# Optimization experiments

Measured on AMD Instinct MI355X. Metric: run time of the kernel, lower is better.

## Reference

```python
import jax, jax.numpy as jnp
import numpy as np
from jax import lax

B, S, D, H, L = 2, 2048, 512, 512, 2
M, NC, K, NH, WIN = 64, 16, 4, 8, 256
MAX_LR = 0.1


def setup_inputs() -> dict:
    key = jax.random.key(0)
    keys = iter(jax.random.split(key, 40))
    def nrm(shape, scale=0.02):
        return jax.random.normal(next(keys), shape, dtype=jnp.float32) * scale
    p = {}
    p['x'] = jax.random.normal(next(keys), (B, S, D), dtype=jnp.float32)
    p['meta_memory'] = nrm((M, D), 0.05)
    p['mem_w_in'] = nrm((D, H)); p['mem_b_in'] = jnp.zeros((H,))
    p['mem_w_h'] = nrm((L, H, H)); p['mem_b_h'] = jnp.zeros((L, H))
    p['mem_w_out'] = nrm((H, D)); p['mem_b_out'] = jnp.zeros((D,))
    for n in ('w_in', 'b_in', 'w_h', 'b_h', 'w_out', 'b_out'):
        p['mom_' + n] = jnp.zeros_like(p['mem_' + n])
    for pre in ('q', 'k', 'v'):
        p[pre + '_w'] = nrm((D, D)); p[pre + '_b'] = jnp.zeros((D,))
        p[pre + '_conv'] = nrm((D, 1, K), 0.1)
    for pre in ('lr', 'fg', 'mo'):
        p[pre + '_w'] = nrm((D, 1)); p[pre + '_b'] = jnp.zeros((1,))
    for n in ('swa_wq', 'swa_wk', 'swa_wv', 'swa_wo'):
        p[n] = nrm((D, D))
    for n in ('swa_bq', 'swa_bk', 'swa_bv', 'swa_bo'):
        p[n] = jnp.zeros((D,))
    return p


def l2n(x):
    # F.normalize(x, dim=-1): x / max(||x||_2, 1e-12)
    return x / jnp.maximum(jnp.linalg.norm(x, axis=-1, keepdims=True), 1e-12)


def causal_dwconv(x, kernel):
    # x [B,S,D], kernel [D,1,K] depthwise causal conv along S
    xc = jnp.transpose(x, (0, 2, 1))  # [B,D,S]
    y = lax.conv_general_dilated(xc, kernel, window_strides=(1,), padding=[(K - 1, 0)],
                                 feature_group_count=D, dimension_numbers=('NCH', 'OIH', 'NCH'))
    return jnp.transpose(y, (0, 2, 1))


def lin_proj(x, W, b, conv, n_chunks):
    # Linear -> causal depthwise conv -> SiLU -> chunk: [B, n_chunks, S/n_chunks, D]
    y = jax.nn.silu(causal_dwconv(x @ W + b, conv))
    Bx, Sx, Dx = y.shape
    return y.reshape(Bx, n_chunks, Sx // n_chunks, Dx)


def adaptive(x, W, b, max_w):
    # data-dependent scalar gate in (0, max_w], chunked: [B, NC, chunk_len, 1]
    y = jax.nn.sigmoid(x @ W + b) * max_w
    Bx, Sx, _ = y.shape
    return y.reshape(Bx, NC, Sx // NC, 1)


def mlp(params, x):
    # ResLinear: in-proj + SiLU, residual SiLU hidden layers, out-proj
    h = jax.nn.silu(x @ params['w_in'] + params['b_in'])
    def body(h, wb):
        w, b = wb
        return h + jax.nn.silu(h @ w + b), None
    h, _ = lax.scan(body, h, (params['w_h'], params['b_h']))
    return h @ params['w_out'] + params['b_out']


def swa_attn(x, wq, bq, wk, bk, wv, bv, wo, bo):
    Bx, Sx, Dx = x.shape
    hd = Dx // NH
    def split(y):
        return jnp.transpose(y.reshape(Bx, Sx, NH, hd), (0, 2, 1, 3))
    q, k, v = split(x @ wq + bq), split(x @ wk + bk), split(x @ wv + bv)
    scores = jnp.einsum('bhqd,bhkd->bhqk', q, k) / np.sqrt(hd).astype(np.float32)
    i = jnp.arange(Sx)[:, None]
    j = jnp.arange(Sx)[None, :]
    mask = (j <= i) & (i - j < WIN)  # causal sliding window
    attn = jax.nn.softmax(jnp.where(mask, scores, jnp.float32(-1e9)), axis=-1)
    out = jnp.einsum('bhqk,bhkd->bhqd', attn, v)
    out = jnp.transpose(out, (0, 2, 1, 3)).reshape(Bx, Sx, Dx)
    return out @ wo + bo


def reference(x, meta_memory, mem_w_in, mem_b_in, mem_w_h, mem_b_h, mem_w_out, mem_b_out,
              mom_w_in, mom_b_in, mom_w_h, mom_b_h, mom_w_out, mom_b_out,
              q_w, q_b, q_conv, k_w, k_b, k_conv, v_w, v_b, v_conv,
              lr_w, lr_b, fg_w, fg_b, mo_w, mo_b,
              swa_wq, swa_bq, swa_wk, swa_bk, swa_wv, swa_bv, swa_wo, swa_bo):
    Bx = x.shape[0]
    # inject meta memory; (M+S) chosen divisible by NC so no padding branch
    xm = jnp.concatenate([jnp.broadcast_to(meta_memory, (Bx, M, D)), x], axis=1)
    q = l2n(lin_proj(xm, q_w, q_b, q_conv, 1))      # [B,1,M+S,D]
    k = l2n(lin_proj(xm, k_w, k_b, k_conv, NC))     # [B,NC,C,D]
    v = lin_proj(xm, v_w, v_b, v_conv, NC)
    lr = adaptive(xm, lr_w, lr_b, MAX_LR)           # [B,NC,C,1]
    fg = adaptive(xm, fg_w, fg_b, 1.0)
    mo = adaptive(xm, mo_w, mo_b, 1.0)
    params = {'w_in': mem_w_in, 'b_in': mem_b_in, 'w_h': mem_w_h, 'b_h': mem_b_h,
              'w_out': mem_w_out, 'b_out': mem_b_out}
    moms = {'w_in': mom_w_in, 'b_in': mom_b_in, 'w_h': mom_w_h, 'b_h': mom_b_h,
            'w_out': mom_w_out, 'b_out': mom_b_out}

    def loss_fn(p, kc, vc, lrc):
        preds = mlp(p, kc)                           # [B,C,D]
        loss = jnp.mean((preds - vc) ** 2, axis=-1)  # [B,C]
        return jnp.sum(loss * lrc[..., 0]), loss

    grads, _ = jax.vmap(jax.grad(loss_fn, has_aux=True), in_axes=(None, 1, 1, 1))(params, k, v, lr)
    alpha = fg.mean(axis=(1, 2, 3))  # [B]
    theta = lr.mean(axis=(1, 2, 3))
    eta = mo.mean(axis=(1, 2, 3))
    new_params = {}
    for name, p_ in params.items():
        g = grads[name].mean(axis=0)                # mean over chunks
        sh = (-1,) + (1,) * g.ndim                  # flatten_and_expand
        mom_b = eta.reshape(sh) * moms[name] - theta.reshape(sh) * g   # [B,*shape]
        # torch updates param.data under no_grad -> stop_gradient for faithfulness
        new_params[name] = lax.stop_gradient((p_ * (1.0 - alpha.reshape(sh)) + mom_b).mean(axis=0))
    retrieved = jax.nn.silu(mlp(new_params, q[:, 0]))
    out = swa_attn(retrieved, swa_wq, swa_bq, swa_wk, swa_bk, swa_wv, swa_bv, swa_wo, swa_bo)
    return out[:, M:, :]
```

## Files before the change

### kernel.cpp

```cpp
#include <hip/hip_runtime.h>
#include <cmath>


namespace {

constexpr int Bb   = 2;
constexpr int Ss   = 2048;
constexpr int Dd   = 512;
constexpr int Mm   = 64;
constexpr int NCc  = 16;
constexpr int NHh  = 8;
constexpr int HD   = 64;
constexpr int WINw = 256;
constexpr int Nn   = Mm + Ss;
constexpr int Rr   = Bb * Nn;
constexpr int NBD  = Rr * Dd;
constexpr float MAXLR = 0.1f;

typedef __attribute__((ext_vector_type(8))) short short8;
typedef __attribute__((ext_vector_type(4))) float f32x4;

__device__ __forceinline__ float sigf(float x)  { return 1.0f / (1.0f + __expf(-x)); }
__device__ __forceinline__ float siluf(float x) { return x * sigf(x); }
__device__ __forceinline__ float dsiluf(float x){ float s = sigf(x); return s * (1.0f + x * (1.0f - s)); }
__device__ __forceinline__ unsigned short f2bf(float f) {
    unsigned int u = __float_as_uint(f);
    u = (u + 0x7FFFu + ((u >> 16) & 1u)) >> 16;
    return (unsigned short)u;
}
__device__ __forceinline__ float bf2f(unsigned short h) {
    return __uint_as_float(((unsigned int)h) << 16);
}
__device__ __forceinline__ int swz(int u) { return u ^ ((u >> 4) & 7); }

__global__ void k_build_xm(const float* __restrict__ x, const float* __restrict__ meta,
                           unsigned short* __restrict__ xh, unsigned short* __restrict__ xl) {
    int i = blockIdx.x * 256 + threadIdx.x;
    if (i >= Rr * 128) return;
    int c = i & 127, r = i >> 7;
    int b = r / Nn, t = r - b * Nn;
    float4 v = (t < Mm) ? ((const float4*)meta)[t * 128 + c]
                        : ((const float4*)x)[(size_t)(b * Ss + (t - Mm)) * 128 + c];
    float vv[4] = { v.x, v.y, v.z, v.w };
    unsigned short h[4], l[4];
    #pragma unroll
    for (int e = 0; e < 4; ++e) { h[e] = f2bf(vv[e]); l[e] = f2bf(vv[e] - bf2f(h[e])); }
    *(ushort4*)(xh + (size_t)i * 4) = *(ushort4*)h;
    *(ushort4*)(xl + (size_t)i * 4) = *(ushort4*)l;
}

__global__ void k_gates(const unsigned short* __restrict__ xh, const unsigned short* __restrict__ xl,
                        const float* __restrict__ lw, const float* __restrict__ lb,
                        const float* __restrict__ fw, const float* __restrict__ fb,
                        const float* __restrict__ mw, const float* __restrict__ mb,
                        float* __restrict__ lr_t, float* __restrict__ fg_t, float* __restrict__ mo_t) {
    int r = blockIdx.x * 4 + (threadIdx.x >> 6);
    int lane = threadIdx.x & 63;
    if (r >= Rr) return;
    float s0 = 0.f, s1 = 0.f, s2 = 0.f;
    for (int j = lane; j < Dd; j += 64) {
        size_t o = (size_t)r * Dd + j;
        float v = bf2f(xh[o]) + bf2f(xl[o]);
        s0 += v * lw[j]; s1 += v * fw[j]; s2 += v * mw[j];
    }
    #pragma unroll
    for (int off = 32; off; off >>= 1) {
        s0 += __shfl_down(s0, off, 64);
        s1 += __shfl_down(s1, off, 64);
        s2 += __shfl_down(s2, off, 64);
    }
    if (lane == 0) {
        lr_t[r] = MAXLR * sigf(s0 + lb[0]);
        fg_t[r] = sigf(s1 + fb[0]);
        mo_t[r] = sigf(s2 + mb[0]);
    }
}

__global__ void k_gate_means(const float* __restrict__ lr_t, const float* __restrict__ fg_t,
                             const float* __restrict__ mo_t, float* __restrict__ scal) {
    __shared__ float red[256];
    const float* ptrs[3] = { fg_t, lr_t, mo_t };
    for (int w = 0; w < 3; ++w) {
        float acc = 0.f;
        for (int i = threadIdx.x; i < Rr; i += 256) acc += ptrs[w][i];
        red[threadIdx.x] = acc; __syncthreads();
        for (int off = 128; off; off >>= 1) {
            if (threadIdx.x < off) red[threadIdx.x] += red[threadIdx.x + off];
            __syncthreads();
        }
        if (threadIdx.x == 0) scal[w] = red[0] / (float)Rr;
        __syncthreads();
    }
}

struct WC { const float* w[11]; unsigned short* th[11]; unsigned short* tl[11]; unsigned short* nh[11]; };
__global__ void k_wconv(WC wc) {
    int seg = blockIdx.y;
    int i0 = blockIdx.x * 1024 + threadIdx.x * 4;
    float4 v4 = *(const float4*)(wc.w[seg] + i0);
    float vals[4] = { v4.x, v4.y, v4.z, v4.w };
    int r = i0 >> 9, c = i0 & 511;
    #pragma unroll
    for (int e = 0; e < 4; ++e) {
        unsigned short h = f2bf(vals[e]);
        unsigned short l = f2bf(vals[e] - bf2f(h));
        wc.th[seg][(size_t)(c + e) * 512 + r] = h;
        wc.tl[seg][(size_t)(c + e) * 512 + r] = l;
        if (wc.nh[seg]) wc.nh[seg][i0 + e] = h;
    }
}

struct TriW { const unsigned short* bh; const unsigned short* bl; const float* bias; float* c; };
struct TriSet { TriW t[3]; };

template<int TA, int TB, bool SPLITK, int EPI, bool MULTI, int NS, bool AF32>
__global__ __launch_bounds__(256) void k_mm(
        const void* Ap, const unsigned short* Al_,
        const unsigned short* Bh_, const unsigned short* Bl_,
        float* C, const float* bias, const float* __restrict__ exf,
        const unsigned short* __restrict__ exh, const unsigned short* __restrict__ exl,
        const float* __restrict__ lrp,
        unsigned short* oh, unsigned short* ol, TriSet ts,
        int Md, int Nd, int Kd, int accum) {
    constexpr int SMEMB = (NS == 3) ? 32768 : 16384;
    __shared__ char smem[SMEMB];
    unsigned short* AH = (unsigned short*)smem;
    unsigned short* AL = AH + 4096;
    unsigned short* BH = AH + ((NS == 3) ? 8192 : 4096);
    unsigned short* BL = BH + 4096;
    const int tid = threadIdx.x;
    const int m0 = blockIdx.x * 64, n0 = blockIdx.y * 64;
    if constexpr (MULTI) {
        const TriW& tw = ts.t[blockIdx.z];
        Bh_ = tw.bh; Bl_ = tw.bl; bias = tw.bias; C = tw.c;
    }
    int kbg = 0, ke = Kd;
    if constexpr (SPLITK) {
        int kc = Kd / gridDim.z;
        kbg = blockIdx.z * kc; ke = kbg + kc;
        C += (size_t)blockIdx.z * Md * Nd;
    }
    const int astr = (TA == 0) ? Kd : Md;

    f32x4 acc[2][2];
    #pragma unroll
    for (int i = 0; i < 2; ++i)
        #pragma unroll
        for (int j = 0; j < 2; ++j)
            #pragma unroll
            for (int v = 0; v < 4; ++v) acc[i][j][v] = 0.f;

    short8 pA0, pA1, pAl0, pAl1, pB0, pB1, pBl0, pBl1;
    float4 pAf[4];

    auto gload = [&](int k0) {
        if constexpr (TA == 0) {
            int r = tid >> 2, ks2 = (tid & 3) * 16;
            if constexpr (AF32) {
                const float* ap = (const float*)Ap + (size_t)(m0 + r) * astr + k0 + ks2;
                pAf[0] = *(const float4*)ap;       pAf[1] = *(const float4*)(ap + 4);
                pAf[2] = *(const float4*)(ap + 8); pAf[3] = *(const float4*)(ap + 12);
            } else {
                const unsigned short* ah = (const unsigned short*)Ap + (size_t)(m0 + r) * astr + k0 + ks2;
                pA0 = *(const short8*)ah; pA1 = *(const short8*)(ah + 8);
                if constexpr (NS == 3) {
                    const unsigned short* al = Al_ + (size_t)(m0 + r) * astr + k0 + ks2;
                    pAl0 = *(const short8*)al; pAl1 = *(const short8*)(al + 8);
                }
            }
        } else {
            int kr = tid >> 2, ms = (tid & 3) * 16;
            const unsigned short* ah = (const unsigned short*)Ap + (size_t)(k0 + kr) * astr + m0 + ms;
            pA0 = *(const short8*)ah; pA1 = *(const short8*)(ah + 8);
            if constexpr (NS == 3) {
                const unsigned short* al = Al_ + (size_t)(k0 + kr) * astr + m0 + ms;
                pAl0 = *(const short8*)al; pAl1 = *(const short8*)(al + 8);
            }
        }
        if constexpr (TB == 0) {
            int nr = tid >> 2, ks2 = (tid & 3) * 16;
            const unsigned short* bh = Bh_ + (size_t)(n0 + nr) * Kd + k0 + ks2;
            pB0 = *(const short8*)bh; pB1 = *(const short8*)(bh + 8);
            if constexpr (NS == 3) {
                const unsigned short* bl = Bl_ + (size_t)(n0 + nr) * Kd + k0 + ks2;
                pBl0 = *(const short8*)bl; pBl1 = *(const short8*)(bl + 8);
            }
        } else {
            int kr = tid >> 2, nseg = (tid & 3) * 16;
            const unsigned short* bh = Bh_ + (size_t)(k0 + kr) * Nd + n0 + nseg;
            pB0 = *(const short8*)bh; pB1 = *(const short8*)(bh + 8);
            if constexpr (NS == 3) {
                const unsigned short* bl = Bl_ + (size_t)(k0 + kr) * Nd + n0 + nseg;
                pBl0 = *(const short8*)bl; pBl1 = *(const short8*)(bl + 8);
            }
        }
    };
    auto lstore = [&]() {
        if constexpr (TA == 0) {
            int r = tid >> 2, ks2 = (tid & 3) * 16;
            int f = r >> 4, rr = r & 15, kf = ks2 >> 5, q = (ks2 >> 3) & 3;
            int F = (f * 2 + kf) * 4 + q;
            int u0 = swz(F * 16 + rr) * 8, u1 = swz((F + 1) * 16 + rr) * 8;
            if constexpr (AF32) {
                unsigned short hh[16], ll[16];
                const float* pf = (const float*)pAf;
                #pragma unroll
                for (int e = 0; e < 16; ++e) { hh[e] = f2bf(pf[e]); ll[e] = f2bf(pf[e] - bf2f(hh[e])); }
                *(short8*)(AH + u0) = *(short8*)hh;  *(short8*)(AH + u1) = *(short8*)(hh + 8);
                *(short8*)(AL + u0) = *(short8*)ll;  *(short8*)(AL + u1) = *(short8*)(ll + 8);
            } else {
                *(short8*)(AH + u0) = pA0; *(short8*)(AH + u1) = pA1;
                if constexpr (NS == 3) { *(short8*)(AL + u0) = pAl0; *(short8*)(AL + u1) = pAl1; }
            }
        } else {
            int kr = tid >> 2, ms = (tid & 3) * 16;
            int f = ms >> 4, kf = kr >> 5, q = (kr >> 3) & 3, kk = kr & 7;
            int F = (f * 2 + kf) * 4 + q;
            unsigned short tmp[16];
            *(short8*)tmp = pA0; *(short8*)(tmp + 8) = pA1;
            #pragma unroll
            for (int e = 0; e < 16; ++e) AH[swz((F << 4) | e) * 8 + kk] = tmp[e];
            if constexpr (NS == 3) {
                *(short8*)tmp = pAl0; *(short8*)(tmp + 8) = pAl1;
                #pragma unroll
                for (int e = 0; e < 16; ++e) AL[swz((F << 4) | e) * 8 + kk] = tmp[e];
            }
        }
        if constexpr (TB == 0) {
            int nr = tid >> 2, ks2 = (tid & 3) * 16;
            int f = nr >> 4, rr = nr & 15, kf = ks2 >> 5, q = (ks2 >> 3) & 3;
            int F = (f * 2 + kf) * 4 + q;
            int u0 = swz(F * 16 + rr) * 8, u1 = swz((F + 1) * 16 + rr) * 8;
            *(short8*)(BH + u0) = pB0; *(short8*)(BH + u1) = pB1;
            if constexpr (NS == 3) { *(short8*)(BL + u0) = pBl0; *(short8*)(BL + u1) = pBl1; }
        } else {
            int kr = tid >> 2, nseg = (tid & 3) * 16;
            int f = nseg >> 4, kf = kr >> 5, q = (kr >> 3) & 3, kk = kr & 7;
            int F = (f * 2 + kf) * 4 + q;
            unsigned short tmp[16];
            *(short8*)tmp = pB0; *(short8*)(tmp + 8) = pB1;
            #pragma unroll
            for (int e = 0; e < 16; ++e) BH[swz((F << 4) | e) * 8 + kk] = tmp[e];
            if constexpr (NS == 3) {
                *(short8*)tmp = pBl0; *(short8*)(tmp + 8) = pBl1;
                #pragma unroll
                for (int e = 0; e < 16; ++e) BL[swz((F << 4) | e) * 8 + kk] = tmp[e];
            }
        }
    };

    const int wv = tid >> 6, lr16 = tid & 15, lq = (tid >> 4) & 3;
    const int wm = wv & 1, wn = wv >> 1;

    gload(kbg); lstore();
    __syncthreads();
    for (int k0 = kbg; k0 < ke; k0 += 64) {
        bool more = (k0 + 64) < ke;
        if (more) gload(k0 + 64);
        #pragma unroll
        for (int kf = 0; kf < 2; ++kf) {
            short8 fa[2], fal[2], fb[2], fbl[2];
            #pragma unroll
            for (int i = 0; i < 2; ++i) {
                int fA = wm * 2 + i;
                int u = swz(((fA * 2 + kf) * 4 + lq) * 16 + lr16);
                fa[i] = *(const short8*)(AH + u * 8);
                if constexpr (NS == 3) fal[i] = *(const short8*)(AL + u * 8);
            }
            #pragma unroll
            for (int j = 0; j < 2; ++j) {
                int fB = wn * 2 + j;
                int u = swz(((fB * 2 + kf) * 4 + lq) * 16 + lr16);
                fb[j] = *(const short8*)(BH + u * 8);
                if constexpr (NS == 3) fbl[j] = *(const short8*)(BL + u * 8);
            }
            #pragma unroll
            for (int i = 0; i < 2; ++i)
                #pragma unroll
                for (int j = 0; j < 2; ++j) {
                    acc[i][j] = __builtin_amdgcn_mfma_f32_16x16x32_bf16(fa[i], fb[j], acc[i][j], 0, 0, 0);
                    if constexpr (NS == 3) {
                        acc[i][j] = __builtin_amdgcn_mfma_f32_16x16x32_bf16(fa[i], fbl[j], acc[i][j], 0, 0, 0);
                        acc[i][j] = __builtin_amdgcn_mfma_f32_16x16x32_bf16(fal[i], fb[j], acc[i][j], 0, 0, 0);
                    }
                }
        }
        if (more) { __syncthreads(); lstore(); __syncthreads(); }
    }
    __syncthreads();

    float* EP = (float*)smem;
    #pragma unroll
    for (int i = 0; i < 2; ++i)
        #pragma unroll
        for (int j = 0; j < 2; ++j)
            #pragma unroll
            for (int v = 0; v < 4; ++v) {
                int row = wm * 32 + i * 16 + lq * 4 + v;
                int col = wn * 32 + j * 16 + lr16;
                int u = col >> 2, up = u ^ (row & 15);
                EP[row * 64 + up * 4 + (col & 3)] = acc[i][j][v];
            }
    __syncthreads();
    int r = tid >> 2, cg = tid & 3;
    float vv[16];
    #pragma unroll
    for (int uu = 0; uu < 4; ++uu) {
        int u = cg * 4 + uu;
        *(float4*)&vv[uu * 4] = *(const float4*)&EP[r * 64 + ((u ^ (r & 15)) * 4)];
    }
    int m = m0 + r, nb = n0 + cg * 16;
    size_t idx = (size_t)m * Nd + nb;

    if constexpr (SPLITK) {
        #pragma unroll
        for (int uu = 0; uu < 4; ++uu) *(float4*)(C + idx + uu * 4) = *(float4*)&vv[uu * 4];
        return;
    }
    if (bias) {
        #pragma unroll
        for (int uu = 0; uu < 4; ++uu) {
            float4 b4 = *(const float4*)(bias + nb + uu * 4);
            vv[uu * 4 + 0] += b4.x; vv[uu * 4 + 1] += b4.y;
            vv[uu * 4 + 2] += b4.z; vv[uu * 4 + 3] += b4.w;
        }
    }
    unsigned short eh8[16], el8[16];
    if constexpr (EPI == 2 || EPI == 3 || EPI == 6) {
        #pragma unroll
        for (int k4 = 0; k4 < 2; ++k4) {
            *(short8*)&eh8[k4 * 8] = *(const short8*)(exh + idx + k4 * 8);
            *(short8*)&el8[k4 * 8] = *(const short8*)(exl + idx + k4 * 8);
        }
    }
    auto store_hl = [&](const float* s) {
        unsigned short hb[16], lb2[16];
        #pragma unroll
        for (int e = 0; e < 16; ++e) { hb[e] = f2bf(s[e]); lb2[e] = f2bf(s[e] - bf2f(hb[e])); }
        #pragma unroll
        for (int k4 = 0; k4 < 2; ++k4) {
            *(short8*)(oh + idx + k4 * 8) = *(short8*)&hb[k4 * 8];
            *(short8*)(ol + idx + k4 * 8) = *(short8*)&lb2[k4 * 8];
        }
    };
    auto accum_add = [&]() {
        #pragma unroll
        for (int uu = 0; uu < 4; ++uu) {
            float4 o4 = *(const float4*)(C + idx + uu * 4);
            vv[uu * 4 + 0] += o4.x; vv[uu * 4 + 1] += o4.y;
            vv[uu * 4 + 2] += o4.z; vv[uu * 4 + 3] += o4.w;
        }
    };
    auto store_f = [&]() {
        #pragma unroll
        for (int uu = 0; uu < 4; ++uu) *(float4*)(C + idx + uu * 4) = *(float4*)&vv[uu * 4];
    };
    if constexpr (EPI == 0) {
        if (accum) accum_add();
        store_f();
    } else if constexpr (EPI == 1) {
        float s[16];
        #pragma unroll
        for (int e = 0; e < 16; ++e) s[e] = siluf(vv[e]);
        store_hl(s);
    } else if constexpr (EPI == 2) {
        float s[16];
        #pragma unroll
        for (int e = 0; e < 16; ++e) s[e] = bf2f(eh8[e]) + bf2f(el8[e]) + siluf(vv[e]);
        store_hl(s);
    } else if constexpr (EPI == 3) {
        float sc = (2.0f / 512.0f) * lrp[m];
        float s[16];
        #pragma unroll
        for (int e = 0; e < 16; ++e) s[e] = sc * (vv[e] - (bf2f(eh8[e]) + bf2f(el8[e])));
        store_hl(s);
    } else if constexpr (EPI == 4) {
        if (accum) accum_add();
        store_f();
        float s[16];
        #pragma unroll
        for (int e = 0; e < 16; ++e) s[e] = vv[e] * dsiluf(exf[idx + e]);
        store_hl(s);
    } else if constexpr (EPI == 5) {
        store_f();
        float s[16];
        #pragma unroll
        for (int e = 0; e < 16; ++e) s[e] = siluf(vv[e]);
        store_hl(s);
    } else if constexpr (EPI == 6) {
        store_f();
        float s[16];
        #pragma unroll
        for (int e = 0; e < 16; ++e) s[e] = bf2f(eh8[e]) + bf2f(el8[e]) + siluf(vv[e]);
        store_hl(s);
    } else if constexpr (EPI == 7) {
        int b2 = m / Nn, t2 = m - b2 * Nn;
        if (t2 >= Mm) {
            float* dst = C + (size_t)(b2 * Ss + (t2 - Mm)) * Nd + nb;
            #pragma unroll
            for (int uu = 0; uu < 4; ++uu) *(float4*)(dst + uu * 4) = *(float4*)&vv[uu * 4];
        }
    }
}

__global__ void k_reduce_splitk(const float* __restrict__ part, float* __restrict__ out,
                                int n, int z, float alpha) {
    int i = blockIdx.x * 256 + threadIdx.x;
    if (i >= n) return;
    float s = 0.f;
    for (int zz = 0; zz < z; ++zz) s += part[(size_t)zz * n + i];
    out[i] = alpha * s;
}

__global__ __launch_bounds__(256) void k_conv3(
        const float* __restrict__ yq, const float* __restrict__ yk, const float* __restrict__ yv,
        const float* __restrict__ cq, const float* __restrict__ ck, const float* __restrict__ cv,
        unsigned short* oqh, unsigned short* oql, unsigned short* okh, unsigned short* okl,
        unsigned short* ovh, unsigned short* ovl) {
    int which = blockIdx.y;
    const float* y  = which == 0 ? yq : which == 1 ? yk : yv;
    const float* cw = which == 0 ? cq : which == 1 ? ck : cv;
    unsigned short* oh = which == 0 ? oqh : which == 1 ? okh : ovh;
    unsigned short* ol = which == 0 ? oql : which == 1 ? okl : ovl;
    bool norm = which < 2;
    int r = blockIdx.x;
    int b = r / Nn, t = r - b * Nn;
    const size_t rowbase = (size_t)r * Dd;
    float s[2];
    #pragma unroll
    for (int u = 0; u < 2; ++u) {
        int d = threadIdx.x + u * 256;
        float acc = 0.f;
        #pragma unroll
        for (int k = 0; k < 4; ++k) {
            int tt = t - 3 + k;
            if (tt >= 0) acc += y[(size_t)(b * Nn + tt) * Dd + d] * cw[d * 4 + k];
        }
        s[u] = siluf(acc);
    }
    float denom = 1.0f;
    if (norm) {
        __shared__ float wr[4];
        float v2 = s[0] * s[0] + s[1] * s[1];
        #pragma unroll
        for (int off = 32; off; off >>= 1) v2 += __shfl_xor(v2, off, 64);
        if ((threadIdx.x & 63) == 0) wr[threadIdx.x >> 6] = v2;
        __syncthreads();
        denom = fmaxf(sqrtf(wr[0] + wr[1] + wr[2] + wr[3]), 1e-12f);
    }
    #pragma unroll
    for (int u = 0; u < 2; ++u) {
        float v = s[u] / denom;
        unsigned short h = f2bf(v);
        oh[rowbase + threadIdx.x + u * 256] = h;
        ol[rowbase + threadIdx.x + u * 256] = f2bf(v - bf2f(h));
    }
}

__global__ void k_colsum(const unsigned short* __restrict__ gh, const unsigned short* __restrict__ gl,
                         float* __restrict__ part) {
    int col = blockIdx.x * 256 + threadIdx.x;
    int chunk = blockIdx.y;
    int r0 = chunk * (Rr / 64);
    float s = 0.f;
    for (int r = r0; r < r0 + Rr / 64; ++r) {
        size_t o = (size_t)r * Dd + col;
        s += bf2f(gh[o]) + bf2f(gl[o]);
    }
    part[chunk * Dd + col] = s;
}
__global__ void k_colsum_reduce(const float* __restrict__ part, float* __restrict__ out, float alpha) {
    int col = blockIdx.x * 256 + threadIdx.x;
    if (col >= Dd) return;
    float s = 0.f;
    for (int c = 0; c < 64; ++c) s += part[c * Dd + col];
    out[col] = alpha * s;
}

struct UpdW4 { const float* p[4]; const float* mo[4]; const float* g[4];
               unsigned short* th[4]; unsigned short* tl[4]; };
__global__ void k_updW(UpdW4 u, const float* __restrict__ scal) {
    int seg = blockIdx.y;
    int i0 = blockIdx.x * 1024 + threadIdx.x * 4;
    float4 p4 = *(const float4*)(u.p[seg] + i0);
    float4 m4 = *(const float4*)(u.mo[seg] + i0);
    float4 g4 = *(const float4*)(u.g[seg] + i0);
    float a = 1.0f - scal[0], et = scal[2], th = scal[1];
    float vals[4] = { p4.x * a + et * m4.x - th * g4.x, p4.y * a + et * m4.y - th * g4.y,
                      p4.z * a + et * m4.z - th * g4.z, p4.w * a + et * m4.w - th * g4.w };
    int r = i0 >> 9, c = i0 & 511;
    #pragma unroll
    for (int e = 0; e < 4; ++e) {
        unsigned short h = f2bf(vals[e]);
        u.th[seg][(size_t)(c + e) * 512 + r] = h;
        u.tl[seg][(size_t)(c + e) * 512 + r] = f2bf(vals[e] - bf2f(h));
    }
}
struct UpdB4 { const float* p[4]; const float* mo[4]; const float* g[4]; float* o[4]; };
__global__ void k_updB(UpdB4 u, const float* __restrict__ scal) {
    int seg = blockIdx.x >> 1;
    int i = (blockIdx.x & 1) * 256 + threadIdx.x;
    u.o[seg][i] = u.p[seg][i] * (1.0f - scal[0]) + scal[2] * u.mo[seg][i] - scal[1] * u.g[seg][i];
}

__global__ __launch_bounds__(256) void k_swa(const float* __restrict__ qs,
                                             const float* __restrict__ ks,
                                             const float* __restrict__ vs,
                                             float* __restrict__ out) {
    __shared__ unsigned short KH[2048], KL[2048], VH[2048], VL[2048];
    __shared__ unsigned short PH[4][512], PL[4][512];
    const int tid = threadIdx.x;
    const int w = tid >> 6, lane = tid & 63;
    const int lq = lane >> 4, l16 = lane & 15;
    const int q0 = blockIdx.x * 64;
    const int bh = blockIdx.y;
    const int h = bh & 7, b = bh >> 3;
    const size_t srow = (size_t)(b * Nn) * Dd + h * HD;
    const int iq = q0 + w * 16 + l16;

    short8 qh[2], qlo[2];
    {
        const float* qr = qs + srow + (size_t)iq * Dd;
        #pragma unroll
        for (int kf = 0; kf < 2; ++kf) {
            float t8[8];
            *(float4*)&t8[0] = *(const float4*)(qr + kf * 32 + lq * 8);
            *(float4*)&t8[4] = *(const float4*)(qr + kf * 32 + lq * 8 + 4);
            unsigned short hh[8], ll[8];
            #pragma unroll
            for (int e = 0; e < 8; ++e) { hh[e] = f2bf(t8[e]); ll[e] = f2bf(t8[e] - bf2f(hh[e])); }
            qh[kf] = *(short8*)hh; qlo[kf] = *(short8*)ll;
        }
    }

    f32x4 o[4];
    #pragma unroll
    for (int nf = 0; nf < 4; ++nf)
        #pragma unroll
        for (int v = 0; v < 4; ++v) o[nf][v] = 0.f;
    float mrun[4] = { -1e30f, -1e30f, -1e30f, -1e30f };
    float lrun[4] = { 0.f, 0.f, 0.f, 0.f };
    const int iw = q0 + w * 16 + lq * 4;

    int jlo = q0 - (WINw - 1); if (jlo < 0) jlo = 0;
    jlo &= ~31;
    for (int jt = jlo; jt < q0 + 64; jt += 32) {
        __syncthreads();
        {
            int nr = tid >> 3, ds8 = (tid & 7) * 8;
            const float* kr = ks + srow + (size_t)(jt + nr) * Dd + ds8;
            float t8[8];
            *(float4*)&t8[0] = *(const float4*)kr;
            *(float4*)&t8[4] = *(const float4*)(kr + 4);
            unsigned short hh[8], ll[8];
            #pragma unroll
            for (int e = 0; e < 8; ++e) { hh[e] = f2bf(t8[e]); ll[e] = f2bf(t8[e] - bf2f(hh[e])); }
            int f = nr >> 4, rr = nr & 15, kf = ds8 >> 5, q = (ds8 >> 3) & 3;
            int u = swz(((f * 2 + kf) * 4 + q) * 16 + rr);
            *(short8*)(KH + u * 8) = *(short8*)hh;
            *(short8*)(KL + u * 8) = *(short8*)ll;
        }
        {
            int d = tid & 63, kg = tid >> 6;
            unsigned short hh[8], ll[8];
            #pragma unroll
            for (int e = 0; e < 8; ++e) {
                float v = vs[srow + (size_t)(jt + kg * 8 + e) * Dd + d];
                hh[e] = f2bf(v); ll[e] = f2bf(v - bf2f(hh[e]));
            }
            int f = d >> 4, rr = d & 15;
            int u = swz((f * 4 + kg) * 16 + rr);
            *(short8*)(VH + u * 8) = *(short8*)hh;
            *(short8*)(VL + u * 8) = *(short8*)ll;
        }
        __syncthreads();

        f32x4 s[2];
        #pragma unroll
        for (int nf = 0; nf < 2; ++nf) {
            #pragma unroll
            for (int v = 0; v < 4; ++v) s[nf][v] = 0.f;
            #pragma unroll
            for (int kf = 0; kf < 2; ++kf) {
                int u = swz(((nf * 2 + kf) * 4 + lq) * 16 + l16);
                short8 kbh = *(const short8*)(KH + u * 8);
                short8 kbl = *(const short8*)(KL + u * 8);
                s[nf] = __builtin_amdgcn_mfma_f32_16x16x32_bf16(qh[kf], kbh, s[nf], 0, 0, 0);
                s[nf] = __builtin_amdgcn_mfma_f32_16x16x32_bf16(qh[kf], kbl, s[nf], 0, 0, 0);
                s[nf] = __builtin_amdgcn_mfma_f32_16x16x32_bf16(qlo[kf], kbh, s[nf], 0, 0, 0);
            }
        }
        float mt[4];
        #pragma unroll
        for (int v = 0; v < 4; ++v) {
            int i = iw + v;
            int j0c = jt + l16, j1c = jt + 16 + l16;
            s[0][v] = ((j0c <= i) && (i - j0c < WINw)) ? s[0][v] * 0.125f : -1e30f;
            s[1][v] = ((j1c <= i) && (i - j1c < WINw)) ? s[1][v] * 0.125f : -1e30f;
            mt[v] = fmaxf(s[0][v], s[1][v]);
        }
        #pragma unroll
        for (int msk = 1; msk < 16; msk <<= 1)
            #pragma unroll
            for (int v = 0; v < 4; ++v) mt[v] = fmaxf(mt[v], __shfl_xor(mt[v], msk, 64));
        float rs[4];
        #pragma unroll
        for (int v = 0; v < 4; ++v) {
            float mnew = fmaxf(mrun[v], mt[v]);
            float corr = __expf(mrun[v] - mnew);
            mrun[v] = mnew;
            float p0 = (s[0][v] > -1e29f) ? __expf(s[0][v] - mnew) : 0.f;
            float p1 = (s[1][v] > -1e29f) ? __expf(s[1][v] - mnew) : 0.f;
            s[0][v] = p0; s[1][v] = p1;
            rs[v] = p0 + p1;
            lrun[v] *= corr;
            #pragma unroll
            for (int nf = 0; nf < 4; ++nf) o[nf][v] *= corr;
        }
        #pragma unroll
        for (int msk = 1; msk < 16; msk <<= 1)
            #pragma unroll
            for (int v = 0; v < 4; ++v) rs[v] += __shfl_xor(rs[v], msk, 64);
        #pragma unroll
        for (int v = 0; v < 4; ++v) lrun[v] += rs[v];

        #pragma unroll
        for (int nf = 0; nf < 2; ++nf)
            #pragma unroll
            for (int v = 0; v < 4; ++v) {
                float p = s[nf][v];
                unsigned short hh = f2bf(p);
                int row = lq * 4 + v;
                int cu = (nf * 2 + (l16 >> 3)) ^ (row >> 2);
                int addr = row * 32 + cu * 8 + (l16 & 7);
                PH[w][addr] = hh;
                PL[w][addr] = f2bf(p - bf2f(hh));
            }
        __syncthreads();
        int pa = l16 * 32 + (lq ^ (l16 >> 2)) * 8;
        short8 pah = *(const short8*)(&PH[w][pa]);
        short8 pal = *(const short8*)(&PL[w][pa]);
        #pragma unroll
        for (int nf = 0; nf < 4; ++nf) {
            int u = swz((nf * 4 + lq) * 16 + l16);
            short8 vth = *(const short8*)(VH + u * 8);
            short8 vtl = *(const short8*)(VL + u * 8);
            o[nf] = __builtin_amdgcn_mfma_f32_16x16x32_bf16(pah, vth, o[nf], 0, 0, 0);
            o[nf] = __builtin_amdgcn_mfma_f32_16x16x32_bf16(pah, vtl, o[nf], 0, 0, 0);
            o[nf] = __builtin_amdgcn_mfma_f32_16x16x32_bf16(pal, vth, o[nf], 0, 0, 0);
        }
    }
    float invl[4];
    #pragma unroll
    for (int v = 0; v < 4; ++v) invl[v] = 1.0f / lrun[v];
    #pragma unroll
    for (int nf = 0; nf < 4; ++nf)
        #pragma unroll
        for (int v = 0; v < 4; ++v)
            out[srow + (size_t)(iw + v) * Dd + nf * 16 + l16] = o[nf][v] * invl[v];
}

}

extern "C" void kernel_launch(void* const* d_in, const int* in_sizes, int n_in,
                              void* d_out, int out_size, void* d_ws, size_t ws_size,
                              hipStream_t stream) {
    const float* x       = (const float*)d_in[0];
    const float* meta    = (const float*)d_in[1];
    const float* mWin    = (const float*)d_in[2];
    const float* mbin    = (const float*)d_in[3];
    const float* mWh     = (const float*)d_in[4];
    const float* mbh     = (const float*)d_in[5];
    const float* mWout   = (const float*)d_in[6];
    const float* mbout   = (const float*)d_in[7];
    const float* momWin  = (const float*)d_in[8];
    const float* mombin  = (const float*)d_in[9];
    const float* momWh   = (const float*)d_in[10];
    const float* mombh   = (const float*)d_in[11];
    const float* momWout = (const float*)d_in[12];
    const float* mombout = (const float*)d_in[13];
    const float* q_w = (const float*)d_in[14]; const float* q_b = (const float*)d_in[15]; const float* q_c = (const float*)d_in[16];
    const float* k_w = (const float*)d_in[17]; const float* k_b = (const float*)d_in[18]; const float* k_c = (const float*)d_in[19];
    const float* v_w = (const float*)d_in[20]; const float* v_b = (const float*)d_in[21]; const float* v_c = (const float*)d_in[22];
    const float* lr_w = (const float*)d_in[23]; const float* lr_b = (const float*)d_in[24];
    const float* fg_w = (const float*)d_in[25]; const float* fg_b = (const float*)d_in[26];
    const float* mo_w = (const float*)d_in[27]; const float* mo_b = (const float*)d_in[28];
    const float* swa_wq = (const float*)d_in[29]; const float* swa_wk = (const float*)d_in[30];
    const float* swa_wv = (const float*)d_in[31]; const float* swa_wo = (const float*)d_in[32];
    const float* swa_bq = (const float*)d_in[33]; const float* swa_bk = (const float*)d_in[34];
    const float* swa_bv = (const float*)d_in[35]; const float* swa_bo = (const float*)d_in[36];
    (void)in_sizes; (void)n_in; (void)out_size; (void)ws_size;

    char* wsb = (char*)d_ws;
    size_t off = 0;
    auto allocB = [&](size_t bytes) { void* p = wsb + off; off = (off + bytes + 255) & ~(size_t)255; return p; };
    auto allocU = [&](size_t elems) { return (unsigned short*)allocB(elems * 2); };
    auto allocF = [&](size_t elems) { return (float*)allocB(elems * 4); };

    unsigned short *xm_h = allocU(NBD), *xm_l = allocU(NBD);
    unsigned short *qb_h = allocU(NBD), *qb_l = allocU(NBD);
    unsigned short *kb_h = allocU(NBD), *kb_l = allocU(NBD);
    unsigned short *vb_h = allocU(NBD), *vb_l = allocU(NBD);
    unsigned short *h0_h = allocU(NBD), *h0_l = allocU(NBD);
    unsigned short *h1_h = allocU(NBD), *h1_l = allocU(NBD);
    unsigned short *h2_h = allocU(NBD), *h2_l = allocU(NBD);
    unsigned short *g1_h = allocU(NBD), *g1_l = allocU(NBD);
    float *f0 = allocF(NBD), *f1 = allocF(NBD), *f2 = allocF(NBD), *f3 = allocF(NBD);
    float *parts = allocF((size_t)12 * 262144);
    const int WEL = 262144;
    unsigned short *wt_h[11], *wt_l[11], *wn_h[11];
    for (int i = 0; i < 11; ++i) { wt_h[i] = allocU(WEL); wt_l[i] = allocU(WEL); wn_h[i] = nullptr; }
    for (int i = 8; i < 11; ++i) wn_h[i] = allocU(WEL);
    unsigned short *nWinT_h = allocU(WEL), *nWinT_l = allocU(WEL);
    unsigned short *nWh0T_h = allocU(WEL), *nWh0T_l = allocU(WEL);
    unsigned short *nWh1T_h = allocU(WEL), *nWh1T_l = allocU(WEL);
    unsigned short *nWoutT_h = allocU(WEL), *nWoutT_l = allocU(WEL);
    float *gWin = allocF(WEL), *gWh0 = allocF(WEL), *gWh1 = allocF(WEL), *gWout = allocF(WEL);
    float *gbin = allocF(512), *gbh0 = allocF(512), *gbh1 = allocF(512), *gbout = allocF(512);
    float *nbin = allocF(512), *nbh0 = allocF(512), *nbh1 = allocF(512), *nbout = allocF(512);
    float *lr_t = allocF(Rr), *fg_t = allocF(Rr), *mo_t = allocF(Rr);
    float *scal = allocF(8);
    float *cpart = allocF(64 * 512);
    unsigned short *gA_h = vb_h, *gA_l = vb_l;
    unsigned short *gB_h = xm_h, *gB_l = xm_l;

    TriSet none{};
    const dim3 GG(66, 8);

    WC wc{};
    const float* wlist[11] = { q_w, k_w, v_w, swa_wq, swa_wk, swa_wv, swa_wo,
                               mWin, mWh, mWh + WEL, mWout };
    for (int i = 0; i < 11; ++i) { wc.w[i] = wlist[i]; wc.th[i] = wt_h[i]; wc.tl[i] = wt_l[i]; wc.nh[i] = wn_h[i]; }
    k_wconv<<<dim3(256, 11), 256, 0, stream>>>(wc);

    k_build_xm<<<(Rr * 128 + 255) / 256, 256, 0, stream>>>(x, meta, xm_h, xm_l);
    k_gates<<<Rr / 4, 256, 0, stream>>>(xm_h, xm_l, lr_w, lr_b, fg_w, fg_b, mo_w, mo_b, lr_t, fg_t, mo_t);
    k_gate_means<<<1, 256, 0, stream>>>(lr_t, fg_t, mo_t, scal);

    TriSet qkvA{{ { wt_h[0], wt_l[0], q_b, f0 }, { wt_h[1], wt_l[1], k_b, f1 }, { wt_h[2], wt_l[2], v_b, f2 } }};
    k_mm<0, 0, false, 0, true, 3, false><<<dim3(66, 8, 3), 256, 0, stream>>>(
        xm_h, xm_l, nullptr, nullptr, nullptr, nullptr, nullptr, nullptr, nullptr, nullptr,
        nullptr, nullptr, qkvA, Rr, Dd, Dd, 0);
    k_conv3<<<dim3(Rr, 3), 256, 0, stream>>>(f0, f1, f2, q_c, k_c, v_c,
                                             qb_h, qb_l, kb_h, kb_l, vb_h, vb_l);

    k_mm<0, 0, false, 5, false, 1, false><<<GG, 256, 0, stream>>>(
        kb_h, nullptr, wt_h[7], nullptr, f0, mbin, nullptr, nullptr, nullptr, nullptr,
        h0_h, h0_l, none, Rr, Dd, Dd, 0);
    k_mm<0, 0, false, 6, false, 1, false><<<GG, 256, 0, stream>>>(
        h0_h, nullptr, wt_h[8], nullptr, f1, mbh, nullptr, h0_h, h0_l, nullptr,
        h1_h, h1_l, none, Rr, Dd, Dd, 0);
    k_mm<0, 0, false, 6, false, 1, false><<<GG, 256, 0, stream>>>(
        h1_h, nullptr, wt_h[9], nullptr, f2, mbh + 512, nullptr, h1_h, h1_l, nullptr,
        h2_h, h2_l, none, Rr, Dd, Dd, 0);
    k_mm<0, 0, false, 3, false, 1, false><<<GG, 256, 0, stream>>>(
        h2_h, nullptr, wt_h[10], nullptr, nullptr, mbout, nullptr, vb_h, vb_l, lr_t,
        g1_h, g1_l, none, Rr, Dd, Dd, 0);

    auto GRADW = [&](const unsigned short* ah, const unsigned short* bh, float* gout) {
        k_mm<1, 1, true, 0, false, 1, false><<<dim3(8, 8, 11), 256, 0, stream>>>(
            ah, nullptr, bh, nullptr, parts, nullptr, nullptr, nullptr, nullptr, nullptr,
            nullptr, nullptr, none, Dd, Dd, Rr, 0);
        k_reduce_splitk<<<1024, 256, 0, stream>>>(parts, gout, WEL, 11, 1.0f / NCc);
    };
    auto COLSUM = [&](const unsigned short* gh, const unsigned short* gl, float* bo) {
        k_colsum<<<dim3(2, 64), 256, 0, stream>>>(gh, gl, cpart);
        k_colsum_reduce<<<2, 256, 0, stream>>>(cpart, bo, 1.0f / NCc);
    };
    GRADW(h2_h, g1_h, gWout);  COLSUM(g1_h, g1_l, gbout);
    k_mm<0, 0, false, 4, false, 1, false><<<GG, 256, 0, stream>>>(
        g1_h, nullptr, wn_h[10], nullptr, f3, nullptr, f2, nullptr, nullptr, nullptr,
        gA_h, gA_l, none, Rr, Dd, Dd, 0);
    GRADW(h1_h, gA_h, gWh1);   COLSUM(gA_h, gA_l, gbh1);
    k_mm<0, 0, false, 4, false, 1, false><<<GG, 256, 0, stream>>>(
        gA_h, nullptr, wn_h[9], nullptr, f3, nullptr, f1, nullptr, nullptr, nullptr,
        gB_h, gB_l, none, Rr, Dd, Dd, 1);
    GRADW(h0_h, gB_h, gWh0);   COLSUM(gB_h, gB_l, gbh0);
    k_mm<0, 0, false, 4, false, 1, false><<<GG, 256, 0, stream>>>(
        gB_h, nullptr, wn_h[8], nullptr, f3, nullptr, f0, nullptr, nullptr, nullptr,
        gA_h, gA_l, none, Rr, Dd, Dd, 1);
    GRADW(kb_h, gA_h, gWin);   COLSUM(gA_h, gA_l, gbin);

    UpdW4 uw{ { mWin, mWh, mWh + WEL, mWout },
              { momWin, momWh, momWh + WEL, momWout },
              { gWin, gWh0, gWh1, gWout },
              { nWinT_h, nWh0T_h, nWh1T_h, nWoutT_h },
              { nWinT_l, nWh0T_l, nWh1T_l, nWoutT_l } };
    k_updW<<<dim3(256, 4), 256, 0, stream>>>(uw, scal);
    UpdB4 ub{ { mbin, mbh, mbh + 512, mbout },
              { mombin, mombh, mombh + 512, mombout },
              { gbin, gbh0, gbh1, gbout },
              { nbin, nbh0, nbh1, nbout } };
    k_updB<<<8, 256, 0, stream>>>(ub, scal);

    k_mm<0, 0, false, 1, false, 3, false><<<GG, 256, 0, stream>>>(
        qb_h, qb_l, nWinT_h, nWinT_l, nullptr, nbin, nullptr, nullptr, nullptr, nullptr,
        g1_h, g1_l, none, Rr, Dd, Dd, 0);
    k_mm<0, 0, false, 2, false, 3, false><<<GG, 256, 0, stream>>>(
        g1_h, g1_l, nWh0T_h, nWh0T_l, nullptr, nbh0, nullptr, g1_h, g1_l, nullptr,
        h0_h, h0_l, none, Rr, Dd, Dd, 0);
    k_mm<0, 0, false, 2, false, 3, false><<<GG, 256, 0, stream>>>(
        h0_h, h0_l, nWh1T_h, nWh1T_l, nullptr, nbh1, nullptr, h0_h, h0_l, nullptr,
        h1_h, h1_l, none, Rr, Dd, Dd, 0);
    k_mm<0, 0, false, 1, false, 3, false><<<GG, 256, 0, stream>>>(
        h1_h, h1_l, nWoutT_h, nWoutT_l, nullptr, nbout, nullptr, nullptr, nullptr, nullptr,
        h2_h, h2_l, none, Rr, Dd, Dd, 0);

    TriSet qkvF{{ { wt_h[3], wt_l[3], swa_bq, f0 }, { wt_h[4], wt_l[4], swa_bk, f1 },
                  { wt_h[5], wt_l[5], swa_bv, f2 } }};
    k_mm<0, 0, false, 0, true, 3, false><<<dim3(66, 8, 3), 256, 0, stream>>>(
        h2_h, h2_l, nullptr, nullptr, nullptr, nullptr, nullptr, nullptr, nullptr, nullptr,
        nullptr, nullptr, qkvF, Rr, Dd, Dd, 0);
    k_swa<<<dim3(Nn / 64, Bb * NHh), 256, 0, stream>>>(f0, f1, f2, f3);
    k_mm<0, 0, false, 7, false, 3, true><<<GG, 256, 0, stream>>>(
        f3, nullptr, wt_h[6], wt_l[6], (float*)d_out, swa_bo, nullptr, nullptr, nullptr, nullptr,
        nullptr, nullptr, none, Rr, Dd, Dd, 0);
}
```

Before: 638.5 us.

## Replace split-bf16 three-pass GEMMs with single-pass fp16 MFMA and scaled gradients

Drops the hi/lo bf16 split representation everywhere and stores activations and weights as a single fp16 array, using one fp16 MFMA per tile instead of three bf16 MFMAs. Gradients are pre-scaled by a constant factor to stay inside fp16 range, and the weight conversion kernel becomes a shared-memory tiled transpose. This cuts memory traffic and matrix-core work, in exchange for fp16 precision (about 11 mantissa bits), which may lose accuracy compared with the split-bf16 scheme.

```diff
diff --git a/kernel.cpp b/kernel.cpp
--- a/kernel.cpp
+++ b/kernel.cpp
@@ -16,25 +16,26 @@
 constexpr int Rr   = Bb * Nn;
 constexpr int NBD  = Rr * Dd;
 constexpr float MAXLR = 0.1f;
+constexpr float GS   = 256.0f;
 
 typedef __attribute__((ext_vector_type(8))) short short8;
+typedef __attribute__((ext_vector_type(8))) _Float16 half8;
 typedef __attribute__((ext_vector_type(4))) float f32x4;
 
 __device__ __forceinline__ float sigf(float x)  { return 1.0f / (1.0f + __expf(-x)); }
 __device__ __forceinline__ float siluf(float x) { return x * sigf(x); }
 __device__ __forceinline__ float dsiluf(float x){ float s = sigf(x); return s * (1.0f + x * (1.0f - s)); }
-__device__ __forceinline__ unsigned short f2bf(float f) {
-    unsigned int u = __float_as_uint(f);
-    u = (u + 0x7FFFu + ((u >> 16) & 1u)) >> 16;
-    return (unsigned short)u;
-}
-__device__ __forceinline__ float bf2f(unsigned short h) {
-    return __uint_as_float(((unsigned int)h) << 16);
+__device__ __forceinline__ unsigned short f2h(float f) {
+    _Float16 h = (_Float16)f;
+    return *(unsigned short*)&h;
+}
+__device__ __forceinline__ float h2f(unsigned short u) {
+    return (float)(*(_Float16*)&u);
 }
 __device__ __forceinline__ int swz(int u) { return u ^ ((u >> 4) & 7); }
 
 __global__ void k_build_xm(const float* __restrict__ x, const float* __restrict__ meta,
-                           unsigned short* __restrict__ xh, unsigned short* __restrict__ xl) {
+                           unsigned short* __restrict__ xh) {
     int i = blockIdx.x * 256 + threadIdx.x;
     if (i >= Rr * 128) return;
     int c = i & 127, r = i >> 7;
@@ -42,14 +43,13 @@
     float4 v = (t < Mm) ? ((const float4*)meta)[t * 128 + c]
                         : ((const float4*)x)[(size_t)(b * Ss + (t - Mm)) * 128 + c];
     float vv[4] = { v.x, v.y, v.z, v.w };
-    unsigned short h[4], l[4];
-    #pragma unroll
-    for (int e = 0; e < 4; ++e) { h[e] = f2bf(vv[e]); l[e] = f2bf(vv[e] - bf2f(h[e])); }
+    unsigned short h[4];
+    #pragma unroll
+    for (int e = 0; e < 4; ++e) h[e] = f2h(vv[e]);
     *(ushort4*)(xh + (size_t)i * 4) = *(ushort4*)h;
-    *(ushort4*)(xl + (size_t)i * 4) = *(ushort4*)l;
-}
-
-__global__ void k_gates(const unsigned short* __restrict__ xh, const unsigned short* __restrict__ xl,
+}
+
+__global__ void k_gates(const unsigned short* __restrict__ xh,
                         const float* __restrict__ lw, const float* __restrict__ lb,
                         const float* __restrict__ fw, const float* __restrict__ fb,
                         const float* __restrict__ mw, const float* __restrict__ mb,
@@ -59,8 +59,7 @@
     if (r >= Rr) return;
     float s0 = 0.f, s1 = 0.f, s2 = 0.f;
     for (int j = lane; j < Dd; j += 64) {
-        size_t o = (size_t)r * Dd + j;
-        float v = bf2f(xh[o]) + bf2f(xl[o]);
+        float v = h2f(xh[(size_t)r * Dd + j]);
         s0 += v * lw[j]; s1 += v * fw[j]; s2 += v * mw[j];
     }
     #pragma unroll
@@ -93,46 +92,53 @@
     }
 }
 
-struct WC { const float* w[11]; unsigned short* th[11]; unsigned short* tl[11]; unsigned short* nh[11]; };
-__global__ void k_wconv(WC wc) {
-    int seg = blockIdx.y;
-    int i0 = blockIdx.x * 1024 + threadIdx.x * 4;
-    float4 v4 = *(const float4*)(wc.w[seg] + i0);
-    float vals[4] = { v4.x, v4.y, v4.z, v4.w };
-    int r = i0 >> 9, c = i0 & 511;
-    #pragma unroll
-    for (int e = 0; e < 4; ++e) {
-        unsigned short h = f2bf(vals[e]);
-        unsigned short l = f2bf(vals[e] - bf2f(h));
-        wc.th[seg][(size_t)(c + e) * 512 + r] = h;
-        wc.tl[seg][(size_t)(c + e) * 512 + r] = l;
-        if (wc.nh[seg]) wc.nh[seg][i0 + e] = h;
-    }
-}
-
-struct TriW { const unsigned short* bh; const unsigned short* bl; const float* bias; float* c; };
+struct WC { const float* w[11]; unsigned short* th[11]; unsigned short* nh[11]; };
+__global__ __launch_bounds__(256) void k_wconv(WC wc) {
+    __shared__ float T[64][65];
+    int seg = blockIdx.z;
+    int r0 = blockIdx.y * 64, c0 = blockIdx.x * 64;
+    int tr = threadIdx.x >> 2, tc = (threadIdx.x & 3) * 16;
+    const float* wsrc = wc.w[seg] + (size_t)(r0 + tr) * 512 + c0 + tc;
+    float vals[16];
+    #pragma unroll
+    for (int q = 0; q < 4; ++q) *(float4*)&vals[q * 4] = *(const float4*)(wsrc + q * 4);
+    #pragma unroll
+    for (int e = 0; e < 16; ++e) T[tr][tc + e] = vals[e];
+    if (wc.nh[seg]) {
+        unsigned short nh16[16];
+        #pragma unroll
+        for (int e = 0; e < 16; ++e) nh16[e] = f2h(vals[e]);
+        unsigned short* np = wc.nh[seg] + (size_t)(r0 + tr) * 512 + c0 + tc;
+        *(short8*)np = *(short8*)nh16; *(short8*)(np + 8) = *(short8*)(nh16 + 8);
+    }
+    __syncthreads();
+    int c = threadIdx.x >> 2, rb = (threadIdx.x & 3) * 16;
+    unsigned short o16[16];
+    #pragma unroll
+    for (int e = 0; e < 16; ++e) o16[e] = f2h(T[rb + e][c]);
+    unsigned short* tp = wc.th[seg] + (size_t)(c0 + c) * 512 + r0 + rb;
+    *(short8*)tp = *(short8*)o16; *(short8*)(tp + 8) = *(short8*)(o16 + 8);
+}
+
+struct TriW { const unsigned short* bh; const float* bias; float* c; };
 struct TriSet { TriW t[3]; };
 
-template<int TA, int TB, bool SPLITK, int EPI, bool MULTI, int NS, bool AF32>
+template<int TA, int TB, bool SPLITK, int EPI, bool MULTI, bool AF32>
 __global__ __launch_bounds__(256) void k_mm(
-        const void* Ap, const unsigned short* Al_,
-        const unsigned short* Bh_, const unsigned short* Bl_,
+        const void* Ap, const unsigned short* Bh_,
         float* C, const float* bias, const float* __restrict__ exf,
-        const unsigned short* __restrict__ exh, const unsigned short* __restrict__ exl,
+        const unsigned short* __restrict__ exh,
         const float* __restrict__ lrp,
-        unsigned short* oh, unsigned short* ol, TriSet ts,
+        unsigned short* oh, TriSet ts,
         int Md, int Nd, int Kd, int accum) {
-    constexpr int SMEMB = (NS == 3) ? 32768 : 16384;
-    __shared__ char smem[SMEMB];
+    __shared__ char smem[16384];
     unsigned short* AH = (unsigned short*)smem;
-    unsigned short* AL = AH + 4096;
-    unsigned short* BH = AH + ((NS == 3) ? 8192 : 4096);
-    unsigned short* BL = BH + 4096;
+    unsigned short* BH = AH + 4096;
     const int tid = threadIdx.x;
     const int m0 = blockIdx.x * 64, n0 = blockIdx.y * 64;
     if constexpr (MULTI) {
         const TriW& tw = ts.t[blockIdx.z];
-        Bh_ = tw.bh; Bl_ = tw.bl; bias = tw.bias; C = tw.c;
+        Bh_ = tw.bh; bias = tw.bias; C = tw.c;
     }
     int kbg = 0, ke = Kd;
     if constexpr (SPLITK) {
@@ -150,7 +156,7 @@
             #pragma unroll
             for (int v = 0; v < 4; ++v) acc[i][j][v] = 0.f;
 
-    short8 pA0, pA1, pAl0, pAl1, pB0, pB1, pBl0, pBl1;
+    short8 pA0, pA1, pB0, pB1;
     float4 pAf[4];
 
     auto gload = [&](int k0) {
@@ -163,36 +169,20 @@
             } else {
                 const unsigned short* ah = (const unsigned short*)Ap + (size_t)(m0 + r) * astr + k0 + ks2;
                 pA0 = *(const short8*)ah; pA1 = *(const short8*)(ah + 8);
-                if constexpr (NS == 3) {
-                    const unsigned short* al = Al_ + (size_t)(m0 + r) * astr + k0 + ks2;
-                    pAl0 = *(const short8*)al; pAl1 = *(const short8*)(al + 8);
-                }
             }
         } else {
             int kr = tid >> 2, ms = (tid & 3) * 16;
             const unsigned short* ah = (const unsigned short*)Ap + (size_t)(k0 + kr) * astr + m0 + ms;
             pA0 = *(const short8*)ah; pA1 = *(const short8*)(ah + 8);
-            if constexpr (NS == 3) {
-                const unsigned short* al = Al_ + (size_t)(k0 + kr) * astr + m0 + ms;
-                pAl0 = *(const short8*)al; pAl1 = *(const short8*)(al + 8);
-            }
         }
         if constexpr (TB == 0) {
             int nr = tid >> 2, ks2 = (tid & 3) * 16;
             const unsigned short* bh = Bh_ + (size_t)(n0 + nr) * Kd + k0 + ks2;
             pB0 = *(const short8*)bh; pB1 = *(const short8*)(bh + 8);
-            if constexpr (NS == 3) {
-                const unsigned short* bl = Bl_ + (size_t)(n0 + nr) * Kd + k0 + ks2;
-                pBl0 = *(const short8*)bl; pBl1 = *(const short8*)(bl + 8);
-            }
         } else {
             int kr = tid >> 2, nseg = (tid & 3) * 16;
             const unsigned short* bh = Bh_ + (size_t)(k0 + kr) * Nd + n0 + nseg;
             pB0 = *(const short8*)bh; pB1 = *(const short8*)(bh + 8);
-            if constexpr (NS == 3) {
-                const unsigned short* bl = Bl_ + (size_t)(k0 + kr) * Nd + n0 + nseg;
-                pBl0 = *(const short8*)bl; pBl1 = *(const short8*)(bl + 8);
-            }
         }
     };
     auto lstore = [&]() {
@@ -202,15 +192,13 @@
             int F = (f * 2 + kf) * 4 + q;
             int u0 = swz(F * 16 + rr) * 8, u1 = swz((F + 1) * 16 + rr) * 8;
             if constexpr (AF32) {
-                unsigned short hh[16], ll[16];
+                unsigned short hh[16];
                 const float* pf = (const float*)pAf;
                 #pragma unroll
-                for (int e = 0; e < 16; ++e) { hh[e] = f2bf(pf[e]); ll[e] = f2bf(pf[e] - bf2f(hh[e])); }
+                for (int e = 0; e < 16; ++e) hh[e] = f2h(pf[e]);
                 *(short8*)(AH + u0) = *(short8*)hh;  *(short8*)(AH + u1) = *(short8*)(hh + 8);
-                *(short8*)(AL + u0) = *(short8*)ll;  *(short8*)(AL + u1) = *(short8*)(ll + 8);
             } else {
                 *(short8*)(AH + u0) = pA0; *(short8*)(AH + u1) = pA1;
-                if constexpr (NS == 3) { *(short8*)(AL + u0) = pAl0; *(short8*)(AL + u1) = pAl1; }
             }
         } else {
             int kr = tid >> 2, ms = (tid & 3) * 16;
@@ -220,11 +208,6 @@
             *(short8*)tmp = pA0; *(short8*)(tmp + 8) = pA1;
             #pragma unroll
             for (int e = 0; e < 16; ++e) AH[swz((F << 4) | e) * 8 + kk] = tmp[e];
-            if constexpr (NS == 3) {
-                *(short8*)tmp = pAl0; *(short8*)(tmp + 8) = pAl1;
-                #pragma unroll
-                for (int e = 0; e < 16; ++e) AL[swz((F << 4) | e) * 8 + kk] = tmp[e];
-            }
         }
         if constexpr (TB == 0) {
             int nr = tid >> 2, ks2 = (tid & 3) * 16;
@@ -232,7 +215,6 @@
             int F = (f * 2 + kf) * 4 + q;
             int u0 = swz(F * 16 + rr) * 8, u1 = swz((F + 1) * 16 + rr) * 8;
             *(short8*)(BH + u0) = pB0; *(short8*)(BH + u1) = pB1;
-            if constexpr (NS == 3) { *(short8*)(BL + u0) = pBl0; *(short8*)(BL + u1) = pBl1; }
         } else {
             int kr = tid >> 2, nseg = (tid & 3) * 16;
             int f = nseg >> 4, kf = kr >> 5, q = (kr >> 3) & 3, kk = kr & 7;
@@ -241,11 +223,6 @@
             *(short8*)tmp = pB0; *(short8*)(tmp + 8) = pB1;
             #pragma unroll
             for (int e = 0; e < 16; ++e) BH[swz((F << 4) | e) * 8 + kk] = tmp[e];
-            if constexpr (NS == 3) {
-                *(short8*)tmp = pBl0; *(short8*)(tmp + 8) = pBl1;
-                #pragma unroll
-                for (int e = 0; e < 16; ++e) BL[swz((F << 4) | e) * 8 + kk] = tmp[e];
-            }
         }
     };
 
@@ -259,31 +236,22 @@
         if (more) gload(k0 + 64);
         #pragma unroll
         for (int kf = 0; kf < 2; ++kf) {
-            short8 fa[2], fal[2], fb[2], fbl[2];
+            half8 fa[2], fb[2];
             #pragma unroll
             for (int i = 0; i < 2; ++i) {
-                int fA = wm * 2 + i;
-                int u = swz(((fA * 2 + kf) * 4 + lq) * 16 + lr16);
-                fa[i] = *(const short8*)(AH + u * 8);
-                if constexpr (NS == 3) fal[i] = *(const short8*)(AL + u * 8);
+                int u = swz((((wm * 2 + i) * 2 + kf) * 4 + lq) * 16 + lr16);
+                fa[i] = *(const half8*)(AH + u * 8);
             }
             #pragma unroll
             for (int j = 0; j < 2; ++j) {
-                int fB = wn * 2 + j;
-                int u = swz(((fB * 2 + kf) * 4 + lq) * 16 + lr16);
-                fb[j] = *(const short8*)(BH + u * 8);
-                if constexpr (NS == 3) fbl[j] = *(const short8*)(BL + u * 8);
+                int u = swz((((wn * 2 + j) * 2 + kf) * 4 + lq) * 16 + lr16);
+                fb[j] = *(const half8*)(BH + u * 8);
             }
             #pragma unroll
             for (int i = 0; i < 2; ++i)
                 #pragma unroll
-                for (int j = 0; j < 2; ++j) {
-                    acc[i][j] = __builtin_amdgcn_mfma_f32_16x16x32_bf16(fa[i], fb[j], acc[i][j], 0, 0, 0);
-                    if constexpr (NS == 3) {
-                        acc[i][j] = __builtin_amdgcn_mfma_f32_16x16x32_bf16(fa[i], fbl[j], acc[i][j], 0, 0, 0);
-                        acc[i][j] = __builtin_amdgcn_mfma_f32_16x16x32_bf16(fal[i], fb[j], acc[i][j], 0, 0, 0);
-                    }
-                }
+                for (int j = 0; j < 2; ++j)
+                    acc[i][j] = __builtin_amdgcn_mfma_f32_16x16x32_f16(fa[i], fb[j], acc[i][j], 0, 0, 0);
         }
         if (more) { __syncthreads(); lstore(); __syncthreads(); }
     }
@@ -325,23 +293,18 @@
             vv[uu * 4 + 2] += b4.z; vv[uu * 4 + 3] += b4.w;
         }
     }
-    unsigned short eh8[16], el8[16];
+    unsigned short eh8[16];
     if constexpr (EPI == 2 || EPI == 3 || EPI == 6) {
         #pragma unroll
-        for (int k4 = 0; k4 < 2; ++k4) {
+        for (int k4 = 0; k4 < 2; ++k4)
             *(short8*)&eh8[k4 * 8] = *(const short8*)(exh + idx + k4 * 8);
-            *(short8*)&el8[k4 * 8] = *(const short8*)(exl + idx + k4 * 8);
-        }
-    }
-    auto store_hl = [&](const float* s) {
-        unsigned short hb[16], lb2[16];
-        #pragma unroll
-        for (int e = 0; e < 16; ++e) { hb[e] = f2bf(s[e]); lb2[e] = f2bf(s[e] - bf2f(hb[e])); }
-        #pragma unroll
-        for (int k4 = 0; k4 < 2; ++k4) {
-            *(short8*)(oh + idx + k4 * 8) = *(short8*)&hb[k4 * 8];
-            *(short8*)(ol + idx + k4 * 8) = *(short8*)&lb2[k4 * 8];
-        }
+    }
+    auto store_h = [&](const float* s) {
+        unsigned short hb[16];
+        #pragma unroll
+        for (int e = 0; e < 16; ++e) hb[e] = f2h(s[e]);
+        *(short8*)(oh + idx) = *(short8*)hb;
+        *(short8*)(oh + idx + 8) = *(short8*)(hb + 8);
     };
     auto accum_add = [&]() {
         #pragma unroll
@@ -362,37 +325,37 @@
         float s[16];
         #pragma unroll
         for (int e = 0; e < 16; ++e) s[e] = siluf(vv[e]);
-        store_hl(s);
+        store_h(s);
     } else if constexpr (EPI == 2) {
         float s[16];
         #pragma unroll
-        for (int e = 0; e < 16; ++e) s[e] = bf2f(eh8[e]) + bf2f(el8[e]) + siluf(vv[e]);
-        store_hl(s);
+        for (int e = 0; e < 16; ++e) s[e] = h2f(eh8[e]) + siluf(vv[e]);
+        store_h(s);
     } else if constexpr (EPI == 3) {
-        float sc = (2.0f / 512.0f) * lrp[m];
+        float sc = GS * (2.0f / 512.0f) * lrp[m];
         float s[16];
         #pragma unroll
-        for (int e = 0; e < 16; ++e) s[e] = sc * (vv[e] - (bf2f(eh8[e]) + bf2f(el8[e])));
-        store_hl(s);
+        for (int e = 0; e < 16; ++e) s[e] = sc * (vv[e] - h2f(eh8[e]));
+        store_h(s);
     } else if constexpr (EPI == 4) {
         if (accum) accum_add();
         store_f();
         float s[16];
         #pragma unroll
         for (int e = 0; e < 16; ++e) s[e] = vv[e] * dsiluf(exf[idx + e]);
-        store_hl(s);
+        store_h(s);
     } else if constexpr (EPI == 5) {
         store_f();
         float s[16];
         #pragma unroll
         for (int e = 0; e < 16; ++e) s[e] = siluf(vv[e]);
-        store_hl(s);
+        store_h(s);
     } else if constexpr (EPI == 6) {
         store_f();
         float s[16];
         #pragma unroll
-        for (int e = 0; e < 16; ++e) s[e] = bf2f(eh8[e]) + bf2f(el8[e]) + siluf(vv[e]);
-        store_hl(s);
+        for (int e = 0; e < 16; ++e) s[e] = h2f(eh8[e]) + siluf(vv[e]);
+        store_h(s);
     } else if constexpr (EPI == 7) {
         int b2 = m / Nn, t2 = m - b2 * Nn;
         if (t2 >= Mm) {
@@ -415,13 +378,11 @@
 __global__ __launch_bounds__(256) void k_conv3(
         const float* __restrict__ yq, const float* __restrict__ yk, const float* __restrict__ yv,
         const float* __restrict__ cq, const float* __restrict__ ck, const float* __restrict__ cv,
-        unsigned short* oqh, unsigned short* oql, unsigned short* okh, unsigned short* okl,
-        unsigned short* ovh, unsigned short* ovl) {
+        unsigned short* oq, unsigned short* ok, unsigned short* ov) {
     int which = blockIdx.y;
     const float* y  = which == 0 ? yq : which == 1 ? yk : yv;
     const float* cw = which == 0 ? cq : which == 1 ? ck : cv;
-    unsigned short* oh = which == 0 ? oqh : which == 1 ? okh : ovh;
-    unsigned short* ol = which == 0 ? oql : which == 1 ? okl : ovl;
+    unsigned short* oh = which == 0 ? oq : which == 1 ? ok : ov;
     bool norm = which < 2;
     int r = blockIdx.x;
     int b = r / Nn, t = r - b * Nn;
@@ -448,25 +409,16 @@
         __syncthreads();
         denom = fmaxf(sqrtf(wr[0] + wr[1] + wr[2] + wr[3]), 1e-12f);
     }
-    #pragma unroll
-    for (int u = 0; u < 2; ++u) {
-        float v = s[u] / denom;
-        unsigned short h = f2bf(v);
-        oh[rowbase + threadIdx.x + u * 256] = h;
-        ol[rowbase + threadIdx.x + u * 256] = f2bf(v - bf2f(h));
-    }
-}
-
-__global__ void k_colsum(const unsigned short* __restrict__ gh, const unsigned short* __restrict__ gl,
-                         float* __restrict__ part) {
+    oh[rowbase + threadIdx.x]       = f2h(s[0] / denom);
+    oh[rowbase + threadIdx.x + 256] = f2h(s[1] / denom);
+}
+
+__global__ void k_colsum(const unsigned short* __restrict__ gh, float* __restrict__ part) {
     int col = blockIdx.x * 256 + threadIdx.x;
     int chunk = blockIdx.y;
     int r0 = chunk * (Rr / 64);
     float s = 0.f;
-    for (int r = r0; r < r0 + Rr / 64; ++r) {
-        size_t o = (size_t)r * Dd + col;
-        s += bf2f(gh[o]) + bf2f(gl[o]);
-    }
+    for (int r = r0; r < r0 + Rr / 64; ++r) s += h2f(gh[(size_t)r * Dd + col]);
     part[chunk * Dd + col] = s;
 }
 __global__ void k_colsum_reduce(const float* __restrict__ part, float* __restrict__ out, float alpha) {
@@ -477,24 +429,31 @@
     out[col] = alpha * s;
 }
 
-struct UpdW4 { const float* p[4]; const float* mo[4]; const float* g[4];
-               unsigned short* th[4]; unsigned short* tl[4]; };
-__global__ void k_updW(UpdW4 u, const float* __restrict__ scal) {
-    int seg = blockIdx.y;
-    int i0 = blockIdx.x * 1024 + threadIdx.x * 4;
-    float4 p4 = *(const float4*)(u.p[seg] + i0);
-    float4 m4 = *(const float4*)(u.mo[seg] + i0);
-    float4 g4 = *(const float4*)(u.g[seg] + i0);
+struct UpdW4 { const float* p[4]; const float* mo[4]; const float* g[4]; unsigned short* th[4]; };
+__global__ __launch_bounds__(256) void k_updW(UpdW4 u, const float* __restrict__ scal) {
+    __shared__ float T[64][65];
+    int seg = blockIdx.z;
+    int r0 = blockIdx.y * 64, c0 = blockIdx.x * 64;
     float a = 1.0f - scal[0], et = scal[2], th = scal[1];
-    float vals[4] = { p4.x * a + et * m4.x - th * g4.x, p4.y * a + et * m4.y - th * g4.y,
-                      p4.z * a + et * m4.z - th * g4.z, p4.w * a + et * m4.w - th * g4.w };
-    int r = i0 >> 9, c = i0 & 511;
-    #pragma unroll
-    for (int e = 0; e < 4; ++e) {
-        unsigned short h = f2bf(vals[e]);
-        u.th[seg][(size_t)(c + e) * 512 + r] = h;
-        u.tl[seg][(size_t)(c + e) * 512 + r] = f2bf(vals[e] - bf2f(h));
-    }
+    int tr = threadIdx.x >> 2, tc = (threadIdx.x & 3) * 16;
+    size_t base = (size_t)(r0 + tr) * 512 + c0 + tc;
+    #pragma unroll
+    for (int q = 0; q < 4; ++q) {
+        float4 p4 = *(const float4*)(u.p[seg] + base + q * 4);
+        float4 m4 = *(const float4*)(u.mo[seg] + base + q * 4);
+        float4 g4 = *(const float4*)(u.g[seg] + base + q * 4);
+        T[tr][tc + q * 4 + 0] = p4.x * a + et * m4.x - th * g4.x;
+        T[tr][tc + q * 4 + 1] = p4.y * a + et * m4.y - th * g4.y;
+        T[tr][tc + q * 4 + 2] = p4.z * a + et * m4.z - th * g4.z;
+        T[tr][tc + q * 4 + 3] = p4.w * a + et * m4.w - th * g4.w;
+    }
+    __syncthreads();
+    int c = threadIdx.x >> 2, rb = (threadIdx.x & 3) * 16;
+    unsigned short o16[16];
+    #pragma unroll
+    for (int e = 0; e < 16; ++e) o16[e] = f2h(T[rb + e][c]);
+    unsigned short* tp = u.th[seg] + (size_t)(c0 + c) * 512 + r0 + rb;
+    *(short8*)tp = *(short8*)o16; *(short8*)(tp + 8) = *(short8*)(o16 + 8);
 }
 struct UpdB4 { const float* p[4]; const float* mo[4]; const float* g[4]; float* o[4]; };
 __global__ void k_updB(UpdB4 u, const float* __restrict__ scal) {
@@ -507,8 +466,8 @@
                                              const float* __restrict__ ks,
                                              const float* __restrict__ vs,
                                              float* __restrict__ out) {
-    __shared__ unsigned short KH[2048], KL[2048], VH[2048], VL[2048];
-    __shared__ unsigned short PH[4][512], PL[4][512];
+    __shared__ unsigned short KH[2048], VH[2048];
+    __shared__ unsigned short PH[4][512];
     const int tid = threadIdx.x;
     const int w = tid >> 6, lane = tid & 63;
     const int lq = lane >> 4, l16 = lane & 15;
@@ -518,7 +477,7 @@
     const size_t srow = (size_t)(b * Nn) * Dd + h * HD;
     const int iq = q0 + w * 16 + l16;
 
-    short8 qh[2], qlo[2];
+    half8 qh[2];
     {
         const float* qr = qs + srow + (size_t)iq * Dd;
         #pragma unroll
@@ -526,10 +485,10 @@
             float t8[8];
             *(float4*)&t8[0] = *(const float4*)(qr + kf * 32 + lq * 8);
             *(float4*)&t8[4] = *(const float4*)(qr + kf * 32 + lq * 8 + 4);
-            unsigned short hh[8], ll[8];
-            #pragma unroll
-            for (int e = 0; e < 8; ++e) { hh[e] = f2bf(t8[e]); ll[e] = f2bf(t8[e] - bf2f(hh[e])); }
-            qh[kf] = *(short8*)hh; qlo[kf] = *(short8*)ll;
+            unsigned short hh[8];
+            #pragma unroll
+            for (int e = 0; e < 8; ++e) hh[e] = f2h(t8[e]);
+            qh[kf] = *(half8*)hh;
         }
     }
 
@@ -552,26 +511,22 @@
             float t8[8];
             *(float4*)&t8[0] = *(const float4*)kr;
             *(float4*)&t8[4] = *(const float4*)(kr + 4);
-            unsigned short hh[8], ll[8];
-            #pragma unroll
-            for (int e = 0; e < 8; ++e) { hh[e] = f2bf(t8[e]); ll[e] = f2bf(t8[e] - bf2f(hh[e])); }
+            unsigned short hh[8];
+            #pragma unroll
+            for (int e = 0; e < 8; ++e) hh[e] = f2h(t8[e]);
             int f = nr >> 4, rr = nr & 15, kf = ds8 >> 5, q = (ds8 >> 3) & 3;
             int u = swz(((f * 2 + kf) * 4 + q) * 16 + rr);
             *(short8*)(KH + u * 8) = *(short8*)hh;
-            *(short8*)(KL + u * 8) = *(short8*)ll;
         }
         {
             int d = tid & 63, kg = tid >> 6;
-            unsigned short hh[8], ll[8];
-            #pragma unroll
-            for (int e = 0; e < 8; ++e) {
-                float v = vs[srow + (size_t)(jt + kg * 8 + e) * Dd + d];
-                hh[e] = f2bf(v); ll[e] = f2bf(v - bf2f(hh[e]));
-            }
+            unsigned short hh[8];
+            #pragma unroll
+            for (int e = 0; e < 8; ++e)
+                hh[e] = f2h(vs[srow + (size_t)(jt + kg * 8 + e) * Dd + d]);
             int f = d >> 4, rr = d & 15;
             int u = swz((f * 4 + kg) * 16 + rr);
             *(short8*)(VH + u * 8) = *(short8*)hh;
-            *(short8*)(VL + u * 8) = *(short8*)ll;
         }
         __syncthreads();
 
@@ -583,11 +538,8 @@
             #pragma unroll
             for (int kf = 0; kf < 2; ++kf) {
                 int u = swz(((nf * 2 + kf) * 4 + lq) * 16 + l16);
-                short8 kbh = *(const short8*)(KH + u * 8);
-                short8 kbl = *(const short8*)(KL + u * 8);
-                s[nf] = __builtin_amdgcn_mfma_f32_16x16x32_bf16(qh[kf], kbh, s[nf], 0, 0, 0);
-                s[nf] = __builtin_amdgcn_mfma_f32_16x16x32_bf16(qh[kf], kbl, s[nf], 0, 0, 0);
-                s[nf] = __builtin_amdgcn_mfma_f32_16x16x32_bf16(qlo[kf], kbh, s[nf], 0, 0, 0);
+                half8 kb = *(const half8*)(KH + u * 8);
+                s[nf] = __builtin_amdgcn_mfma_f32_16x16x32_f16(qh[kf], kb, s[nf], 0, 0, 0);
             }
         }
         float mt[4];
@@ -628,26 +580,18 @@
         for (int nf = 0; nf < 2; ++nf)
             #pragma unroll
             for (int v = 0; v < 4; ++v) {
-                float p = s[nf][v];
-                unsigned short hh = f2bf(p);
                 int row = lq * 4 + v;
                 int cu = (nf * 2 + (l16 >> 3)) ^ (row >> 2);
-                int addr = row * 32 + cu * 8 + (l16 & 7);
-                PH[w][addr] = hh;
-                PL[w][addr] = f2bf(p - bf2f(hh));
+                PH[w][row * 32 + cu * 8 + (l16 & 7)] = f2h(s[nf][v]);
             }
         __syncthreads();
         int pa = l16 * 32 + (lq ^ (l16 >> 2)) * 8;
-        short8 pah = *(const short8*)(&PH[w][pa]);
-        short8 pal = *(const short8*)(&PL[w][pa]);
+        half8 pah = *(const half8*)(&PH[w][pa]);
         #pragma unroll
         for (int nf = 0; nf < 4; ++nf) {
             int u = swz((nf * 4 + lq) * 16 + l16);
-            short8 vth = *(const short8*)(VH + u * 8);
-            short8 vtl = *(const short8*)(VL + u * 8);
-            o[nf] = __builtin_amdgcn_mfma_f32_16x16x32_bf16(pah, vth, o[nf], 0, 0, 0);
-            o[nf] = __builtin_amdgcn_mfma_f32_16x16x32_bf16(pah, vtl, o[nf], 0, 0, 0);
-            o[nf] = __builtin_amdgcn_mfma_f32_16x16x32_bf16(pal, vth, o[nf], 0, 0, 0);
+            half8 vth = *(const half8*)(VH + u * 8);
+            o[nf] = __builtin_amdgcn_mfma_f32_16x16x32_f16(pah, vth, o[nf], 0, 0, 0);
         }
     }
     float invl[4];
@@ -697,122 +641,105 @@
     auto allocU = [&](size_t elems) { return (unsigned short*)allocB(elems * 2); };
     auto allocF = [&](size_t elems) { return (float*)allocB(elems * 4); };
 
-    unsigned short *xm_h = allocU(NBD), *xm_l = allocU(NBD);
-    unsigned short *qb_h = allocU(NBD), *qb_l = allocU(NBD);
-    unsigned short *kb_h = allocU(NBD), *kb_l = allocU(NBD);
-    unsigned short *vb_h = allocU(NBD), *vb_l = allocU(NBD);
-    unsigned short *h0_h = allocU(NBD), *h0_l = allocU(NBD);
-    unsigned short *h1_h = allocU(NBD), *h1_l = allocU(NBD);
-    unsigned short *h2_h = allocU(NBD), *h2_l = allocU(NBD);
-    unsigned short *g1_h = allocU(NBD), *g1_l = allocU(NBD);
+    unsigned short *xm_h = allocU(NBD);
+    unsigned short *qb_h = allocU(NBD);
+    unsigned short *kb_h = allocU(NBD);
+    unsigned short *vb_h = allocU(NBD);
+    unsigned short *h0_h = allocU(NBD);
+    unsigned short *h1_h = allocU(NBD);
+    unsigned short *h2_h = allocU(NBD);
+    unsigned short *g1_h = allocU(NBD);
     float *f0 = allocF(NBD), *f1 = allocF(NBD), *f2 = allocF(NBD), *f3 = allocF(NBD);
     float *parts = allocF((size_t)12 * 262144);
     const int WEL = 262144;
-    unsigned short *wt_h[11], *wt_l[11], *wn_h[11];
-    for (int i = 0; i < 11; ++i) { wt_h[i] = allocU(WEL); wt_l[i] = allocU(WEL); wn_h[i] = nullptr; }
+    unsigned short *wt_h[11], *wn_h[11];
+    for (int i = 0; i < 11; ++i) { wt_h[i] = allocU(WEL); wn_h[i] = nullptr; }
     for (int i = 8; i < 11; ++i) wn_h[i] = allocU(WEL);
-    unsigned short *nWinT_h = allocU(WEL), *nWinT_l = allocU(WEL);
-    unsigned short *nWh0T_h = allocU(WEL), *nWh0T_l = allocU(WEL);
-    unsigned short *nWh1T_h = allocU(WEL), *nWh1T_l = allocU(WEL);
-    unsigned short *nWoutT_h = allocU(WEL), *nWoutT_l = allocU(WEL);
+    unsigned short *nWinT_h = allocU(WEL);
+    unsigned short *nWh0T_h = allocU(WEL);
+    unsigned short *nWh1T_h = allocU(WEL);
+    unsigned short *nWoutT_h = allocU(WEL);
     float *gWin = allocF(WEL), *gWh0 = allocF(WEL), *gWh1 = allocF(WEL), *gWout = allocF(WEL);
     float *gbin = allocF(512), *gbh0 = allocF(512), *gbh1 = allocF(512), *gbout = allocF(512);
     float *nbin = allocF(512), *nbh0 = allocF(512), *nbh1 = allocF(512), *nbout = allocF(512);
     float *lr_t = allocF(Rr), *fg_t = allocF(Rr), *mo_t = allocF(Rr);
     float *scal = allocF(8);
     float *cpart = allocF(64 * 512);
-    unsigned short *gA_h = vb_h, *gA_l = vb_l;
-    unsigned short *gB_h = xm_h, *gB_l = xm_l;
+    unsigned short *gA_h = vb_h;
+    unsigned short *gB_h = xm_h;
 
     TriSet none{};
     const dim3 GG(66, 8);
+    const float GALPHA = 1.0f / (NCc * GS);
 
     WC wc{};
     const float* wlist[11] = { q_w, k_w, v_w, swa_wq, swa_wk, swa_wv, swa_wo,
                                mWin, mWh, mWh + WEL, mWout };
-    for (int i = 0; i < 11; ++i) { wc.w[i] = wlist[i]; wc.th[i] = wt_h[i]; wc.tl[i] = wt_l[i]; wc.nh[i] = wn_h[i]; }
-    k_wconv<<<dim3(256, 11), 256, 0, stream>>>(wc);
-
-    k_build_xm<<<(Rr * 128 + 255) / 256, 256, 0, stream>>>(x, meta, xm_h, xm_l);
-    k_gates<<<Rr / 4, 256, 0, stream>>>(xm_h, xm_l, lr_w, lr_b, fg_w, fg_b, mo_w, mo_b, lr_t, fg_t, mo_t);
+    for (int i = 0; i < 11; ++i) { wc.w[i] = wlist[i]; wc.th[i] = wt_h[i]; wc.nh[i] = wn_h[i]; }
+    k_wconv<<<dim3(8, 8, 11), 256, 0, stream>>>(wc);
+
+    k_build_xm<<<(Rr * 128 + 255) / 256, 256, 0, stream>>>(x, meta, xm_h);
+    k_gates<<<Rr / 4, 256, 0, stream>>>(xm_h, lr_w, lr_b, fg_w, fg_b, mo_w, mo_b, lr_t, fg_t, mo_t);
     k_gate_means<<<1, 256, 0, stream>>>(lr_t, fg_t, mo_t, scal);
 
-    TriSet qkvA{{ { wt_h[0], wt_l[0], q_b, f0 }, { wt_h[1], wt_l[1], k_b, f1 }, { wt_h[2], wt_l[2], v_b, f2 } }};
-    k_mm<0, 0, false, 0, true, 3, false><<<dim3(66, 8, 3), 256, 0, stream>>>(
-        xm_h, xm_l, nullptr, nullptr, nullptr, nullptr, nullptr, nullptr, nullptr, nullptr,
-        nullptr, nullptr, qkvA, Rr, Dd, Dd, 0);
-    k_conv3<<<dim3(Rr, 3), 256, 0, stream>>>(f0, f1, f2, q_c, k_c, v_c,
-                                             qb_h, qb_l, kb_h, kb_l, vb_h, vb_l);
-
-    k_mm<0, 0, false, 5, false, 1, false><<<GG, 256, 0, stream>>>(
-        kb_h, nullptr, wt_h[7], nullptr, f0, mbin, nullptr, nullptr, nullptr, nullptr,
-        h0_h, h0_l, none, Rr, Dd, Dd, 0);
-    k_mm<0, 0, false, 6, false, 1, false><<<GG, 256, 0, stream>>>(
-        h0_h, nullptr, wt_h[8], nullptr, f1, mbh, nullptr, h0_h, h0_l, nullptr,
-        h1_h, h1_l, none, Rr, Dd, Dd, 0);
-    k_mm<0, 0, false, 6, false, 1, false><<<GG, 256, 0, stream>>>(
-        h1_h, nullptr, wt_h[9], nullptr, f2, mbh + 512, nullptr, h1_h, h1_l, nullptr,
-        h2_h, h2_l, none, Rr, Dd, Dd, 0);
-    k_mm<0, 0, false, 3, false, 1, false><<<GG, 256, 0, stream>>>(
-        h2_h, nullptr, wt_h[10], nullptr, nullptr, mbout, nullptr, vb_h, vb_l, lr_t,
-        g1_h, g1_l, none, Rr, Dd, Dd, 0);
+    TriSet qkvA{{ { wt_h[0], q_b, f0 }, { wt_h[1], k_b, f1 }, { wt_h[2], v_b, f2 } }};
+    k_mm<0, 0, false, 0, true, false><<<dim3(66, 8, 3), 256, 0, stream>>>(
+        xm_h, nullptr, nullptr, nullptr, nullptr, nullptr, nullptr, nullptr, qkvA, Rr, Dd, Dd, 0);
+    k_conv3<<<dim3(Rr, 3), 256, 0, stream>>>(f0, f1, f2, q_c, k_c, v_c, qb_h, kb_h, vb_h);
+
+    k_mm<0, 0, false, 5, false, false><<<GG, 256, 0, stream>>>(
+        kb_h, wt_h[7], f0, mbin, nullptr, nullptr, nullptr, h0_h, none, Rr, Dd, Dd, 0);
+    k_mm<0, 0, false, 6, false, false><<<GG, 256, 0, stream>>>(
+        h0_h, wt_h[8], f1, mbh, nullptr, h0_h, nullptr, h1_h, none, Rr, Dd, Dd, 0);
+    k_mm<0, 0, false, 6, false, false><<<GG, 256, 0, stream>>>(
+        h1_h, wt_h[9], f2, mbh + 512, nullptr, h1_h, nullptr, h2_h, none, Rr, Dd, Dd, 0);
+    k_mm<0, 0, false, 3, false, false><<<GG, 256, 0, stream>>>(
+        h2_h, wt_h[10], nullptr, mbout, nullptr, vb_h, lr_t, g1_h, none, Rr, Dd, Dd, 0);
 
     auto GRADW = [&](const unsigned short* ah, const unsigned short* bh, float* gout) {
-        k_mm<1, 1, true, 0, false, 1, false><<<dim3(8, 8, 11), 256, 0, stream>>>(
-            ah, nullptr, bh, nullptr, parts, nullptr, nullptr, nullptr, nullptr, nullptr,
-            nullptr, nullptr, none, Dd, Dd, Rr, 0);
-        k_reduce_splitk<<<1024, 256, 0, stream>>>(parts, gout, WEL, 11, 1.0f / NCc);
+        k_mm<1, 1, true, 0, false, false><<<dim3(8, 8, 11), 256, 0, stream>>>(
+            ah, bh, parts, nullptr, nullptr, nullptr, nullptr, nullptr, none, Dd, Dd, Rr, 0);
+        k_reduce_splitk<<<1024, 256, 0, stream>>>(parts, gout, WEL, 11, GALPHA);
     };
-    auto COLSUM = [&](const unsigned short* gh, const unsigned short* gl, float* bo) {
-        k_colsum<<<dim3(2, 64), 256, 0, stream>>>(gh, gl, cpart);
-        k_colsum_reduce<<<2, 256, 0, stream>>>(cpart, bo, 1.0f / NCc);
+    auto COLSUM = [&](const unsigned short* gh, float* bo) {
+        k_colsum<<<dim3(2, 64), 256, 0, stream>>>(gh, cpart);
+        k_colsum_reduce<<<2, 256, 0, stream>>>(cpart, bo, GALPHA);
     };
-    GRADW(h2_h, g1_h, gWout);  COLSUM(g1_h, g1_l, gbout);
-    k_mm<0, 0, false, 4, false, 1, false><<<GG, 256, 0, stream>>>(
-        g1_h, nullptr, wn_h[10], nullptr, f3, nullptr, f2, nullptr, nullptr, nullptr,
-        gA_h, gA_l, none, Rr, Dd, Dd, 0);
-    GRADW(h1_h, gA_h, gWh1);   COLSUM(gA_h, gA_l, gbh1);
-    k_mm<0, 0, false, 4, false, 1, false><<<GG, 256, 0, stream>>>(
-        gA_h, nullptr, wn_h[9], nullptr, f3, nullptr, f1, nullptr, nullptr, nullptr,
-        gB_h, gB_l, none, Rr, Dd, Dd, 1);
-    GRADW(h0_h, gB_h, gWh0);   COLSUM(gB_h, gB_l, gbh0);
-    k_mm<0, 0, false, 4, false, 1, false><<<GG, 256, 0, stream>>>(
-        gB_h, nullptr, wn_h[8], nullptr, f3, nullptr, f0, nullptr, nullptr, nullptr,
-        gA_h, gA_l, none, Rr, Dd, Dd, 1);
-    GRADW(kb_h, gA_h, gWin);   COLSUM(gA_h, gA_l, gbin);
+    GRADW(h2_h, g1_h, gWout);  COLSUM(g1_h, gbout);
+    k_mm<0, 0, false, 4, false, false><<<GG, 256, 0, stream>>>(
+        g1_h, wn_h[10], f3, nullptr, f2, nullptr, nullptr, gA_h, none, Rr, Dd, Dd, 0);
+    GRADW(h1_h, gA_h, gWh1);   COLSUM(gA_h, gbh1);
+    k_mm<0, 0, false, 4, false, false><<<GG, 256, 0, stream>>>(
+        gA_h, wn_h[9], f3, nullptr, f1, nullptr, nullptr, gB_h, none, Rr, Dd, Dd, 1);
+    GRADW(h0_h, gB_h, gWh0);   COLSUM(gB_h, gbh0);
+    k_mm<0, 0, false, 4, false, false><<<GG, 256, 0, stream>>>(
+        gB_h, wn_h[8], f3, nullptr, f0, nullptr, nullptr, gA_h, none, Rr, Dd, Dd, 1);
+    GRADW(kb_h, gA_h, gWin);   COLSUM(gA_h, gbin);
 
     UpdW4 uw{ { mWin, mWh, mWh + WEL, mWout },
               { momWin, momWh, momWh + WEL, momWout },
               { gWin, gWh0, gWh1, gWout },
-              { nWinT_h, nWh0T_h, nWh1T_h, nWoutT_h },
-              { nWinT_l, nWh0T_l, nWh1T_l, nWoutT_l } };
-    k_updW<<<dim3(256, 4), 256, 0, stream>>>(uw, scal);
+              { nWinT_h, nWh0T_h, nWh1T_h, nWoutT_h } };
+    k_updW<<<dim3(8, 8, 4), 256, 0, stream>>>(uw, scal);
     UpdB4 ub{ { mbin, mbh, mbh + 512, mbout },
               { mombin, mombh, mombh + 512, mombout },
               { gbin, gbh0, gbh1, gbout },
               { nbin, nbh0, nbh1, nbout } };
     k_updB<<<8, 256, 0, stream>>>(ub, scal);
 
-    k_mm<0, 0, false, 1, false, 3, false><<<GG, 256, 0, stream>>>(
-        qb_h, qb_l, nWinT_h, nWinT_l, nullptr, nbin, nullptr, nullptr, nullptr, nullptr,
-        g1_h, g1_l, none, Rr, Dd, Dd, 0);
-    k_mm<0, 0, false, 2, false, 3, false><<<GG, 256, 0, stream>>>(
-        g1_h, g1_l, nWh0T_h, nWh0T_l, nullptr, nbh0, nullptr, g1_h, g1_l, nullptr,
-        h0_h, h0_l, none, Rr, Dd, Dd, 0);
-    k_mm<0, 0, false, 2, false, 3, false><<<GG, 256, 0, stream>>>(
-        h0_h, h0_l, nWh1T_h, nWh1T_l, nullptr, nbh1, nullptr, h0_h, h0_l, nullptr,
-        h1_h, h1_l, none, Rr, Dd, Dd, 0);
-    k_mm<0, 0, false, 1, false, 3, false><<<GG, 256, 0, stream>>>(
-        h1_h, h1_l, nWoutT_h, nWoutT_l, nullptr, nbout, nullptr, nullptr, nullptr, nullptr,
-        h2_h, h2_l, none, Rr, Dd, Dd, 0);
-
-    TriSet qkvF{{ { wt_h[3], wt_l[3], swa_bq, f0 }, { wt_h[4], wt_l[4], swa_bk, f1 },
-                  { wt_h[5], wt_l[5], swa_bv, f2 } }};
-    k_mm<0, 0, false, 0, true, 3, false><<<dim3(66, 8, 3), 256, 0, stream>>>(
-        h2_h, h2_l, nullptr, nullptr, nullptr, nullptr, nullptr, nullptr, nullptr, nullptr,
-        nullptr, nullptr, qkvF, Rr, Dd, Dd, 0);
+    k_mm<0, 0, false, 1, false, false><<<GG, 256, 0, stream>>>(
+        qb_h, nWinT_h, nullptr, nbin, nullptr, nullptr, nullptr, g1_h, none, Rr, Dd, Dd, 0);
+    k_mm<0, 0, false, 2, false, false><<<GG, 256, 0, stream>>>(
+        g1_h, nWh0T_h, nullptr, nbh0, nullptr, g1_h, nullptr, h0_h, none, Rr, Dd, Dd, 0);
+    k_mm<0, 0, false, 2, false, false><<<GG, 256, 0, stream>>>(
+        h0_h, nWh1T_h, nullptr, nbh1, nullptr, h0_h, nullptr, h1_h, none, Rr, Dd, Dd, 0);
+    k_mm<0, 0, false, 1, false, false><<<GG, 256, 0, stream>>>(
+        h1_h, nWoutT_h, nullptr, nbout, nullptr, nullptr, nullptr, h2_h, none, Rr, Dd, Dd, 0);
+
+    TriSet qkvF{{ { wt_h[3], swa_bq, f0 }, { wt_h[4], swa_bk, f1 }, { wt_h[5], swa_bv, f2 } }};
+    k_mm<0, 0, false, 0, true, false><<<dim3(66, 8, 3), 256, 0, stream>>>(
+        h2_h, nullptr, nullptr, nullptr, nullptr, nullptr, nullptr, nullptr, qkvF, Rr, Dd, Dd, 0);
     k_swa<<<dim3(Nn / 64, Bb * NHh), 256, 0, stream>>>(f0, f1, f2, f3);
-    k_mm<0, 0, false, 7, false, 3, true><<<GG, 256, 0, stream>>>(
-        f3, nullptr, wt_h[6], wt_l[6], (float*)d_out, swa_bo, nullptr, nullptr, nullptr, nullptr,
-        nullptr, nullptr, none, Rr, Dd, Dd, 0);
-}
+    k_mm<0, 0, false, 7, false, true><<<GG, 256, 0, stream>>>(
+        f3, wt_h[6], (float*)d_out, swa_bo, nullptr, nullptr, nullptr, nullptr, none, Rr, Dd, Dd, 0);
+}
```

Measured after the change: 512.5 us. 1.25x faster.
